# Kernel optimization log

Measured on AMD Instinct MI355X. Metric: run time of the kernel, lower is better.

Reference implementation:

```python
import jax, jax.numpy as jnp
import numpy as np

B, T, N, D, NH = 4, 256, 8, 128, 4
SCALES = (1, 2, 3, 5)
LAGS = (1, 2, 3)
MLP_H = 32
NL_SCALE = 0.1
CMIN, CMAX = -2.5, 2.0
L_ENC = 2  # num_attn_layers


def _ln(x, g, b, eps=1e-5):
    m = x.mean(-1, keepdims=True)
    v = ((x - m) ** 2).mean(-1, keepdims=True)
    return (x - m) * jax.lax.rsqrt(v + eps) * g + b


def _gelu(x):
    return jax.nn.gelu(x, approximate=False)


def _mha(q, k, v, Wq, bq, Wk, bk, Wv, bv, Wo, bo, nh):
    Bq, Lq, Dm = q.shape
    Lk = k.shape[1]
    hd = Dm // nh
    qh = (q @ Wq.T + bq).reshape(Bq, Lq, nh, hd).transpose(0, 2, 1, 3)
    kh = (k @ Wk.T + bk).reshape(Bq, Lk, nh, hd).transpose(0, 2, 1, 3)
    vh = (v @ Wv.T + bv).reshape(Bq, Lk, nh, hd).transpose(0, 2, 1, 3)
    s = jnp.einsum('bhqd,bhkd->bhqk', qh, kh) / jnp.sqrt(jnp.float32(hd))
    p = jax.nn.softmax(s, axis=-1)
    o = jnp.einsum('bhqk,bhkd->bhqd', p, vh).transpose(0, 2, 1, 3).reshape(Bq, Lq, Dm)
    return o @ Wo.T + bo


def setup_inputs() -> dict:
    key = jax.random.key(0)
    ks = jax.random.split(key, 24)
    def w(k, shape, s=0.02):
        return s * jax.random.normal(k, shape, jnp.float32)
    inp = {}
    inp['visible_states'] = jax.random.uniform(ks[0], (B, T, N), jnp.float32) + 0.05
    inp['state_emb'] = jax.random.normal(ks[1], (B, T, N, D), jnp.float32)
    # LearnedBaseline params
    inp['r5'] = 0.1 * jnp.ones((N,), jnp.float32)
    A = 0.02 * jax.random.normal(ks[2], (N, N), jnp.float32)
    inp['A55'] = A.at[jnp.arange(N), jnp.arange(N)].set(-0.2)
    inp['bl_bias'] = jnp.zeros((N,), jnp.float32)
    inp['nl_W1'] = w(ks[3], (MLP_H, N), 0.1); inp['nl_b1'] = jnp.zeros((MLP_H,), jnp.float32)
    inp['nl_W2'] = w(ks[4], (N, MLP_H), 0.1); inp['nl_b2'] = jnp.zeros((N,), jnp.float32)
    # ResidualEncoder input MLP
    IN_DIM = len(SCALES) * (1 + len(LAGS))  # 16
    inp['mlp_W1'] = w(ks[5], (D, IN_DIM), 0.1); inp['mlp_b1'] = jnp.zeros((D,), jnp.float32)
    inp['mlp_W2'] = w(ks[6], (D, D)); inp['mlp_b2'] = jnp.zeros((D,), jnp.float32)
    inp['mlp_ln_g'] = jnp.ones((D,), jnp.float32); inp['mlp_ln_b'] = jnp.zeros((D,), jnp.float32)
    # ResidualEncoder transformer layers (stacked over L_ENC layers)
    inp['enc_qkv_W'] = w(ks[7], (L_ENC, 3 * D, D)); inp['enc_qkv_b'] = jnp.zeros((L_ENC, 3 * D), jnp.float32)
    inp['enc_out_W'] = w(ks[8], (L_ENC, D, D)); inp['enc_out_b'] = jnp.zeros((L_ENC, D), jnp.float32)
    inp['enc_ln1_g'] = jnp.ones((L_ENC, D), jnp.float32); inp['enc_ln1_b'] = jnp.zeros((L_ENC, D), jnp.float32)
    inp['enc_ff_W1'] = w(ks[9], (L_ENC, 2 * D, D)); inp['enc_ff_b1'] = jnp.zeros((L_ENC, 2 * D), jnp.float32)
    inp['enc_ff_W2'] = w(ks[10], (L_ENC, D, 2 * D)); inp['enc_ff_b2'] = jnp.zeros((L_ENC, D), jnp.float32)
    inp['enc_ln2_g'] = jnp.ones((L_ENC, D), jnp.float32); inp['enc_ln2_b'] = jnp.zeros((L_ENC, D), jnp.float32)
    # CrossAttentionFusion
    inp['ca_Wq'] = w(ks[11], (D, D)); inp['ca_bq'] = jnp.zeros((D,), jnp.float32)
    inp['ca_Wk'] = w(ks[12], (D, D)); inp['ca_bk'] = jnp.zeros((D,), jnp.float32)
    inp['ca_Wv'] = w(ks[13], (D, D)); inp['ca_bv'] = jnp.zeros((D,), jnp.float32)
    inp['ca_Wo'] = w(ks[14], (D, D)); inp['ca_bo'] = jnp.zeros((D,), jnp.float32)
    inp['ca_ln1_g'] = jnp.ones((D,), jnp.float32); inp['ca_ln1_b'] = jnp.zeros((D,), jnp.float32)
    inp['ca_ff_W1'] = w(ks[15], (4 * D, 2 * D)); inp['ca_ff_b1'] = jnp.zeros((4 * D,), jnp.float32)
    inp['ca_ff_W2'] = w(ks[16], (D, 4 * D)); inp['ca_ff_b2'] = jnp.zeros((D,), jnp.float32)
    inp['ca_ln2_g'] = jnp.ones((D,), jnp.float32); inp['ca_ln2_b'] = jnp.zeros((D,), jnp.float32)
    return inp


def _forward(visible_states, state_emb, r5, A55, bl_bias, nl_W1, nl_b1, nl_W2, nl_b2,
             mlp_W1, mlp_b1, mlp_W2, mlp_b2, mlp_ln_g, mlp_ln_b,
             enc_qkv_W, enc_qkv_b, enc_out_W, enc_out_b, enc_ln1_g, enc_ln1_b,
             enc_ff_W1, enc_ff_b1, enc_ff_W2, enc_ff_b2, enc_ln2_g, enc_ln2_b,
             ca_Wq, ca_bq, ca_Wk, ca_bk, ca_Wv, ca_bv, ca_Wo, ca_bo,
             ca_ln1_g, ca_ln1_b, ca_ff_W1, ca_ff_b1, ca_ff_W2, ca_ff_b2,
             ca_ln2_g, ca_ln2_b):
    # ---- LearnedBaseline on x_t = visible_states[:, :-1] ----
    safe = jnp.clip(visible_states, 1e-6, None)
    logx = jnp.log(safe)
    x_t = visible_states[:, :-1]  # (B,T-1,N)
    lin = r5 + jnp.einsum('btn,mn->btm', x_t, A55)
    nl = _gelu(x_t @ nl_W1.T + nl_b1) @ nl_W2.T + nl_b2
    b1 = lin + NL_SCALE * nl + bl_bias  # (B,T-1,N)
    # ---- MultiScaleResidual ----
    res_list = []
    for k in SCALES:
        actual = jnp.clip(logx[:, k:] - logx[:, :-k], CMIN * k, CMAX * k)  # (B,T-k,N)
        bk = b1[:, 0:T - k]
        for i in range(1, k):
            bk = bk + b1[:, i:i + T - k]
        res = actual - bk
        res_list.append(jnp.pad(res, ((0, 0), (0, k), (0, 0))))
    residuals = jnp.stack(res_list, axis=-1)  # (B,T,N,S)
    # ---- ResidualEncoder: takens delays ----
    feats = [residuals] + [jnp.pad(residuals, ((0, 0), (lag, 0), (0, 0), (0, 0)))[:, :T]
                           for lag in LAGS]
    x = jnp.concatenate(feats, axis=-1)  # (B,T,N,16)
    x = _gelu(x @ mlp_W1.T + mlp_b1)
    x = _gelu(x @ mlp_W2.T + mlp_b2)
    x = _ln(x, mlp_ln_g, mlp_ln_b)
    # sinusoidal PE over time
    pos = jnp.arange(T, dtype=jnp.float32)[:, None]
    div = jnp.exp(jnp.arange(0, D, 2, dtype=jnp.float32) * (-jnp.log(10000.0) / D))
    pe = jnp.stack([jnp.sin(pos * div), jnp.cos(pos * div)], axis=-1).reshape(T, D)
    x = x + pe[None, :, None, :]
    # temporal self-attention over (B*N, T, D)
    xt = x.transpose(0, 2, 1, 3).reshape(B * N, T, D)
    for i in range(L_ENC):
        Wq, Wk, Wv = jnp.split(enc_qkv_W[i], 3, axis=0)
        bq, bk_, bv = jnp.split(enc_qkv_b[i], 3)
        a = _mha(xt, xt, xt, Wq, bq, Wk, bk_, Wv, bv, enc_out_W[i], enc_out_b[i], NH)
        xt = _ln(xt + a, enc_ln1_g[i], enc_ln1_b[i])
        ff = _gelu(xt @ enc_ff_W1[i].T + enc_ff_b1[i]) @ enc_ff_W2[i].T + enc_ff_b2[i]
        xt = _ln(xt + ff, enc_ln2_g[i], enc_ln2_b[i])
    residual_emb = xt.reshape(B, N, T, D).transpose(0, 2, 1, 3)  # (B,T,N,D)
    # ---- CrossAttentionFusion ----
    s = state_emb.reshape(B, T * N, D)
    r = residual_emb.reshape(B, T * N, D)
    a = _mha(s, r, r, ca_Wq, ca_bq, ca_Wk, ca_bk, ca_Wv, ca_bv, ca_Wo, ca_bo, NH)
    s = _ln(s + a, ca_ln1_g, ca_ln1_b)
    fused = _gelu(jnp.concatenate([s, r], axis=-1) @ ca_ff_W1.T + ca_ff_b1) @ ca_ff_W2.T + ca_ff_b2
    out = _ln(s + fused, ca_ln2_g, ca_ln2_b)
    return out.reshape(B, T, N, D)


def reference(visible_states, state_emb, r5, A55, bl_bias, nl_W1, nl_b1, nl_W2, nl_b2,
              mlp_W1, mlp_b1, mlp_W2, mlp_b2, mlp_ln_g, mlp_ln_b,
              enc_qkv_W, enc_qkv_b, enc_out_W, enc_out_b, enc_ln1_g, enc_ln1_b,
              enc_ff_W1, enc_ff_b1, enc_ff_W2, enc_ff_b2, enc_ln2_g, enc_ln2_b,
              ca_Wq, ca_bq, ca_Wk, ca_bk, ca_Wv, ca_bv, ca_Wo, ca_bo,
              ca_ln1_g, ca_ln1_b, ca_ff_W1, ca_ff_b1, ca_ff_W2, ca_ff_b2,
              ca_ln2_g, ca_ln2_b):
    return _forward(visible_states, state_emb, r5, A55, bl_bias, nl_W1, nl_b1, nl_W2, nl_b2,
                    mlp_W1, mlp_b1, mlp_W2, mlp_b2, mlp_ln_g, mlp_ln_b,
                    enc_qkv_W, enc_qkv_b, enc_out_W, enc_out_b, enc_ln1_g, enc_ln1_b,
                    enc_ff_W1, enc_ff_b1, enc_ff_W2, enc_ff_b2, enc_ln2_g, enc_ln2_b,
                    ca_Wq, ca_bq, ca_Wk, ca_bk, ca_Wv, ca_bv, ca_Wo, ca_bo,
                    ca_ln1_g, ca_ln1_b, ca_ff_W1, ca_ff_b1, ca_ff_W2, ca_ff_b2,
                    ca_ln2_g, ca_ln2_b)
```

## Files before the change

kernel.cpp:

```cpp
#include <hip/hip_runtime.h>
#include <math.h>

#define B_ 4
#define T_ 256
#define N_ 8
#define D_ 128
#define NH_ 4
#define HD_ 32
#define LENC_ 2
#define MLPH_ 32
#define NL_SCALE_ 0.1f

typedef __bf16 bf16;
typedef __attribute__((ext_vector_type(2))) __bf16 bf16x2;
typedef __attribute__((ext_vector_type(4))) __bf16 bf16x4;
typedef __attribute__((ext_vector_type(8))) __bf16 bf16x8;
typedef __attribute__((ext_vector_type(4))) float f32x4;

__device__ __forceinline__ f32x4 pv_mfma16(bf16x4 a, bf16x4 b, f32x4 c) {
#if __has_builtin(__builtin_amdgcn_mfma_f32_16x16x16_bf16)
    return __builtin_amdgcn_mfma_f32_16x16x16_bf16(a, b, c, 0, 0, 0);
#else
    typedef __attribute__((ext_vector_type(4))) short s4;
    union U { bf16x4 h; s4 s; };
    U ua, ub; ua.h = a; ub.h = b;
    return __builtin_amdgcn_mfma_f32_16x16x16bf16_1k(ua.s, ub.s, c, 0, 0, 0);
#endif
}

__device__ __forceinline__ float gelu_f(float x) {
    return 0.5f * x * (1.0f + erff(x * 0.7071067811865476f));
}

__global__ void k_prep_b1(const float* __restrict__ eqkvW, const float* __restrict__ eoutW,
                          const float* __restrict__ eff1, const float* __restrict__ eff2,
                          const float* __restrict__ wq, const float* __restrict__ wk,
                          const float* __restrict__ wv, const float* __restrict__ wo,
                          const float* __restrict__ cff1, const float* __restrict__ cff2,
                          const float* __restrict__ mlpW2, const float* __restrict__ semb,
                          const float* __restrict__ bk, const float* __restrict__ bv,
                          bf16* __restrict__ Wpk, bf16* __restrict__ sembh,
                          float* __restrict__ bpk,
                          const float* __restrict__ vs, const float* __restrict__ r5,
                          const float* __restrict__ A55, const float* __restrict__ bl_bias,
                          const float* __restrict__ nlW1, const float* __restrict__ nlb1,
                          const float* __restrict__ nlW2, const float* __restrict__ nlb2,
                          float* __restrict__ b1w) {
    if (blockIdx.x < 6209) {
        int i = blockIdx.x * 256 + threadIdx.x;
        if (i < 540672) {
            const float* src; int off;
            if      (i < 98304)  { src = eqkvW; off = 0; }
            else if (i < 131072) { src = eoutW; off = 98304; }
            else if (i < 196608) { src = eff1;  off = 131072; }
            else if (i < 262144) { src = eff2;  off = 196608; }
            else if (i < 278528) { src = wq;    off = 262144; }
            else if (i < 294912) { src = wk;    off = 278528; }
            else if (i < 311296) { src = wv;    off = 294912; }
            else if (i < 327680) { src = wo;    off = 311296; }
            else if (i < 458752) { src = cff1;  off = 327680; }
            else if (i < 524288) { src = cff2;  off = 458752; }
            else                 { src = mlpW2; off = 524288; }
            Wpk[i] = (bf16)src[i - off];
        } else if (i < 540672 + 1048576) {
            int j = i - 540672;
            sembh[j] = (bf16)semb[j];
        } else if (i < 540672 + 1048576 + 256) {
            int t = i - 540672 - 1048576;
            bpk[t] = (t < 128) ? bk[t] : bv[t - 128];
        }
        return;
    }
    int idx = (blockIdx.x - 6209) * 256 + threadIdx.x;
    if (idx >= B_ * (T_ - 1)) return;
    int b = idx / (T_ - 1), t = idx % (T_ - 1);
    float x[N_];
    for (int n = 0; n < N_; n++) x[n] = vs[(b * T_ + t) * N_ + n];
    float h[MLPH_];
    for (int j = 0; j < MLPH_; j++) {
        float a = nlb1[j];
        for (int n = 0; n < N_; n++) a += x[n] * nlW1[j * N_ + n];
        h[j] = gelu_f(a);
    }
    for (int m = 0; m < N_; m++) {
        float lin = r5[m];
        for (int n = 0; n < N_; n++) lin += x[n] * A55[m * N_ + n];
        float nl = nlb2[m];
        for (int j = 0; j < MLPH_; j++) nl += h[j] * nlW2[m * MLPH_ + j];
        b1w[idx * N_ + m] = lin + NL_SCALE_ * nl + bl_bias[m];
    }
}

__global__ __launch_bounds__(256) void k_mlp_ln(
    const float* __restrict__ vs, const float* __restrict__ b1w,
    const float* __restrict__ W1, const float* __restrict__ b1,
    const bf16* __restrict__ W2, const float* __restrict__ bias,
    const float* __restrict__ g, const float* __restrict__ be,
    float* __restrict__ outf, bf16* __restrict__ outh) {
    __shared__ float F[32][16];
    __shared__ bf16 H1[32][136];
    __shared__ float S[32][132];
    int tid = threadIdx.x;
    int blk = blockIdx.x;
#pragma unroll
    for (int e = tid; e < 512; e += 256) {
        int row = e >> 4, feat = e & 15;
        int grow = blk * 32 + row;
        int b = grow >> 11, t = (grow >> 3) & 255, n = grow & 7;
        const int SC[4] = {1, 2, 3, 5};
        int lag = feat >> 2, si = feat & 3, k = SC[si];
        int tp = t - lag;
        float r = 0.0f;
        if (tp >= 0 && tp < T_ - k) {
            float lx0 = logf(fmaxf(vs[(b * T_ + tp) * N_ + n], 1e-6f));
            float lx1 = logf(fmaxf(vs[(b * T_ + tp + k) * N_ + n], 1e-6f));
            float a = lx1 - lx0;
            a = fminf(fmaxf(a, -2.5f * (float)k), 2.0f * (float)k);
            float bk = 0.0f;
            for (int i = 0; i < k; i++) bk += b1w[(b * (T_ - 1) + tp + i) * N_ + n];
            r = a - bk;
        }
        F[row][feat] = r;
    }
    __syncthreads();
    {
        int row = tid >> 3, cg = tid & 7;
        float f[16];
#pragma unroll
        for (int c = 0; c < 16; c++) f[c] = F[row][c];
#pragma unroll
        for (int j = 0; j < 16; j++) {
            int d = cg * 16 + j;
            float a = b1[d];
            const float* w = W1 + d * 16;
#pragma unroll
            for (int c = 0; c < 16; c++) a += f[c] * w[c];
            H1[row][d] = (bf16)gelu_f(a);
        }
    }
    __syncthreads();
    int w = tid >> 6, lane = tid & 63;
    int c = lane & 15, gq = lane >> 4;
    int r0l = (w >> 1) * 16;
    int cb = (w & 1) * 64;
    const f32x4 zero = {0, 0, 0, 0};
    {
        const bf16x8* Wp0 = (const bf16x8*)(W2 + (size_t)(cb + c) * 128) + gq;
        const bf16x8* Wp1 = (const bf16x8*)(W2 + (size_t)(cb + 16 + c) * 128) + gq;
        const bf16x8* Wp2 = (const bf16x8*)(W2 + (size_t)(cb + 32 + c) * 128) + gq;
        const bf16x8* Wp3 = (const bf16x8*)(W2 + (size_t)(cb + 48 + c) * 128) + gq;
        f32x4 a0 = zero, a1 = zero, a2 = zero, a3 = zero;
#pragma unroll
        for (int k = 0; k < 4; k++) {
            bf16x8 av = *(const bf16x8*)&H1[r0l + c][k * 32 + gq * 8];
            a0 = __builtin_amdgcn_mfma_f32_16x16x32_bf16(av, Wp0[k * 4], a0, 0, 0, 0);
            a1 = __builtin_amdgcn_mfma_f32_16x16x32_bf16(av, Wp1[k * 4], a1, 0, 0, 0);
            a2 = __builtin_amdgcn_mfma_f32_16x16x32_bf16(av, Wp2[k * 4], a2, 0, 0, 0);
            a3 = __builtin_amdgcn_mfma_f32_16x16x32_bf16(av, Wp3[k * 4], a3, 0, 0, 0);
        }
        int lrow = r0l + gq * 4;
#pragma unroll
        for (int r = 0; r < 4; r++) {
            S[lrow + r][cb + c]      = gelu_f(a0[r] + bias[cb + c]);
            S[lrow + r][cb + 16 + c] = gelu_f(a1[r] + bias[cb + 16 + c]);
            S[lrow + r][cb + 32 + c] = gelu_f(a2[r] + bias[cb + 32 + c]);
            S[lrow + r][cb + 48 + c] = gelu_f(a3[r] + bias[cb + 48 + c]);
        }
    }
    __syncthreads();
    {
        int row = tid >> 3, cg = tid & 7;
        int grow = blk * 32 + row;
        int b = grow >> 11, t = (grow >> 3) & 255, n = grow & 7;
        int orow = (b * 8 + n) * 256 + t;
        float v[16];
#pragma unroll
        for (int j = 0; j < 16; j++) v[j] = S[row][cg * 16 + j];
        float s = 0.0f;
#pragma unroll
        for (int j = 0; j < 16; j++) s += v[j];
        s += __shfl_xor(s, 1); s += __shfl_xor(s, 2); s += __shfl_xor(s, 4);
        float mean = s * (1.0f / 128.0f);
        float vs2 = 0.0f;
#pragma unroll
        for (int j = 0; j < 16; j++) { float d = v[j] - mean; vs2 += d * d; }
        vs2 += __shfl_xor(vs2, 1); vs2 += __shfl_xor(vs2, 2); vs2 += __shfl_xor(vs2, 4);
        float rstd = rsqrtf(vs2 * (1.0f / 128.0f) + 1e-5f);
        float y[16];
#pragma unroll
        for (int j = 0; j < 16; j++) {
            int col = cg * 16 + j;
            y[j] = (v[j] - mean) * rstd * g[col] + be[col];
        }
#pragma unroll
        for (int jj = 0; jj < 8; jj++) {
            int j2 = cg * 8 + jj;
            float freq = expf((float)(2 * j2) * (-9.210340371976184f / 128.0f));
            float ang = (float)t * freq;
            y[2 * jj] += sinf(ang);
            y[2 * jj + 1] += cosf(ang);
        }
        float4* of = (float4*)(outf + (size_t)orow * 128 + cg * 16);
        bf16x8* oh = (bf16x8*)(outh + (size_t)orow * 128 + cg * 16);
#pragma unroll
        for (int j4 = 0; j4 < 4; j4++) {
            float4 o; o.x = y[4 * j4]; o.y = y[4 * j4 + 1];
            o.z = y[4 * j4 + 2]; o.w = y[4 * j4 + 3];
            of[j4] = o;
        }
#pragma unroll
        for (int j8 = 0; j8 < 2; j8++) {
            bf16x8 o;
#pragma unroll
            for (int e = 0; e < 8; e++) o[e] = (bf16)y[8 * j8 + e];
            oh[j8] = o;
        }
    }
}

__global__ __launch_bounds__(256) void k_enc_attn(
    const bf16* __restrict__ X0h, const bf16* __restrict__ Wqkv,
    const float* __restrict__ bqkv, bf16* __restrict__ ATTh) {
    int sh = blockIdx.x;
    int s = sh >> 2, h = sh & 3;
    __shared__ bf16 Ql[256][40];
    __shared__ bf16 Kl[256][40];
    __shared__ bf16 Vt[32][264];
    int tid = threadIdx.x;
    int wv = tid >> 6, lane = tid & 63;
    int c = lane & 15, g = lane >> 4;
    const f32x4 zero = {0, 0, 0, 0};

    {
        const bf16* Wq0 = Wqkv + (size_t)(h * 32 + c) * 128;
        const bf16* Wq1 = Wqkv + (size_t)(h * 32 + 16 + c) * 128;
        const bf16* Wk0 = Wqkv + (size_t)(128 + h * 32 + c) * 128;
        const bf16* Wk1 = Wqkv + (size_t)(128 + h * 32 + 16 + c) * 128;
        const bf16* Wv0 = Wqkv + (size_t)(256 + h * 32 + c) * 128;
        const bf16* Wv1 = Wqkv + (size_t)(256 + h * 32 + 16 + c) * 128;
        float bq0 = bqkv[h * 32 + c], bq1 = bqkv[h * 32 + 16 + c];
        float bk0 = bqkv[128 + h * 32 + c], bk1 = bqkv[128 + h * 32 + 16 + c];
        float bv0 = bqkv[256 + h * 32 + c], bv1 = bqkv[256 + h * 32 + 16 + c];
#pragma unroll
        for (int rb = 0; rb < 4; rb++) {
            int row0 = wv * 64 + rb * 16;
            const bf16x8* Ap = (const bf16x8*)(X0h + (size_t)(s * 256 + row0 + c) * 128) + g;
            f32x4 aq0 = zero, aq1 = zero, ak0 = zero, ak1 = zero, av0 = zero, av1 = zero;
#pragma unroll
            for (int k = 0; k < 4; k++) {
                bf16x8 av = Ap[k * 4];
                aq0 = __builtin_amdgcn_mfma_f32_16x16x32_bf16(av, *((const bf16x8*)Wq0 + k * 4 + g), aq0, 0, 0, 0);
                aq1 = __builtin_amdgcn_mfma_f32_16x16x32_bf16(av, *((const bf16x8*)Wq1 + k * 4 + g), aq1, 0, 0, 0);
                ak0 = __builtin_amdgcn_mfma_f32_16x16x32_bf16(av, *((const bf16x8*)Wk0 + k * 4 + g), ak0, 0, 0, 0);
                ak1 = __builtin_amdgcn_mfma_f32_16x16x32_bf16(av, *((const bf16x8*)Wk1 + k * 4 + g), ak1, 0, 0, 0);
                av0 = __builtin_amdgcn_mfma_f32_16x16x32_bf16(av, *((const bf16x8*)Wv0 + k * 4 + g), av0, 0, 0, 0);
                av1 = __builtin_amdgcn_mfma_f32_16x16x32_bf16(av, *((const bf16x8*)Wv1 + k * 4 + g), av1, 0, 0, 0);
            }
            int lr = row0 + g * 4;
#pragma unroll
            for (int i = 0; i < 4; i++) {
                Ql[lr + i][c] = (bf16)(aq0[i] + bq0);
                Ql[lr + i][16 + c] = (bf16)(aq1[i] + bq1);
                Kl[lr + i][c] = (bf16)(ak0[i] + bk0);
                Kl[lr + i][16 + c] = (bf16)(ak1[i] + bk1);
                Vt[c][lr + i] = (bf16)(av0[i] + bv0);
                Vt[16 + c][lr + i] = (bf16)(av1[i] + bv1);
            }
        }
    }
    __syncthreads();

    const float scale = 0.17677669529663687f;
    int q0 = wv * 64;
    bf16x8 bq[4];
#pragma unroll
    for (int qt = 0; qt < 4; qt++)
        bq[qt] = *(const bf16x8*)&Ql[q0 + qt * 16 + c][g * 8];
    f32x4 oT[4][2];
#pragma unroll
    for (int qt = 0; qt < 4; qt++) { oT[qt][0] = zero; oT[qt][1] = zero; }
    float lsum[4] = {0, 0, 0, 0};
#pragma unroll
    for (int t = 0; t < 8; t++) {
        int k0 = t * 32;
        bf16x8 ka = *(const bf16x8*)&Kl[k0 + c][g * 8];
        bf16x8 kb = *(const bf16x8*)&Kl[k0 + 16 + c][g * 8];
        bf16x4 va0 = *(const bf16x4*)&Vt[c][k0 + g * 4];
        bf16x4 va1 = *(const bf16x4*)&Vt[c][k0 + 16 + g * 4];
        bf16x4 vb0 = *(const bf16x4*)&Vt[16 + c][k0 + g * 4];
        bf16x4 vb1 = *(const bf16x4*)&Vt[16 + c][k0 + 16 + g * 4];
#pragma unroll
        for (int qt = 0; qt < 4; qt++) {
            f32x4 s0 = __builtin_amdgcn_mfma_f32_16x16x32_bf16(ka, bq[qt], zero, 0, 0, 0);
            f32x4 s1 = __builtin_amdgcn_mfma_f32_16x16x32_bf16(kb, bq[qt], zero, 0, 0, 0);
            bf16x4 p0, p1;
#pragma unroll
            for (int r = 0; r < 4; r++) {
                float e0 = __expf(s0[r] * scale);
                float e1 = __expf(s1[r] * scale);
                lsum[qt] += e0 + e1;
                p0[r] = (bf16)e0;
                p1[r] = (bf16)e1;
            }
            oT[qt][0] = pv_mfma16(va0, p0, oT[qt][0]);
            oT[qt][0] = pv_mfma16(va1, p1, oT[qt][0]);
            oT[qt][1] = pv_mfma16(vb0, p0, oT[qt][1]);
            oT[qt][1] = pv_mfma16(vb1, p1, oT[qt][1]);
        }
    }
#pragma unroll
    for (int qt = 0; qt < 4; qt++) {
        float sm = lsum[qt];
        sm += __shfl_xor(sm, 16);
        sm += __shfl_xor(sm, 32);
        float inv = 1.0f / sm;
        size_t rbase = ((size_t)s * 256 + q0 + qt * 16 + c) * 128 + h * 32;
#pragma unroll
        for (int r = 0; r < 4; r++) {
            ATTh[rbase + g * 4 + r] = (bf16)(oT[qt][0][r] * inv);
            ATTh[rbase + 16 + g * 4 + r] = (bf16)(oT[qt][1][r] * inv);
        }
    }
}

__device__ __forceinline__ void gemm4_body(
    int bid, const bf16* __restrict__ A, const bf16* __restrict__ W,
    const float* __restrict__ bias, bf16* __restrict__ dq,
    bf16* __restrict__ dk, bf16* __restrict__ dvv, int N, int K, int mode) {
    int lane = threadIdx.x & 63;
    int wv = threadIdx.x >> 6;
    int c = lane & 15, g = lane >> 4;
    int nN = N >> 6;
    int tn = bid % nN, tm = bid / nN;
    int row0 = tm * 64 + wv * 16;
    int cb = tn * 64;

    const bf16x8* Ap  = (const bf16x8*)(A + (size_t)(row0 + c) * K) + g;
    const bf16x8* Wp0 = (const bf16x8*)(W + (size_t)(cb + c) * K) + g;
    const bf16x8* Wp1 = (const bf16x8*)(W + (size_t)(cb + 16 + c) * K) + g;
    const bf16x8* Wp2 = (const bf16x8*)(W + (size_t)(cb + 32 + c) * K) + g;
    const bf16x8* Wp3 = (const bf16x8*)(W + (size_t)(cb + 48 + c) * K) + g;
    f32x4 a0 = {0, 0, 0, 0}, a1 = {0, 0, 0, 0};
    f32x4 a2 = {0, 0, 0, 0}, a3 = {0, 0, 0, 0};
    int nk = K >> 5;
    for (int k = 0; k < nk; k++) {
        bf16x8 av = Ap[k * 4];
        a0 = __builtin_amdgcn_mfma_f32_16x16x32_bf16(av, Wp0[k * 4], a0, 0, 0, 0);
        a1 = __builtin_amdgcn_mfma_f32_16x16x32_bf16(av, Wp1[k * 4], a1, 0, 0, 0);
        a2 = __builtin_amdgcn_mfma_f32_16x16x32_bf16(av, Wp2[k * 4], a2, 0, 0, 0);
        a3 = __builtin_amdgcn_mfma_f32_16x16x32_bf16(av, Wp3[k * 4], a3, 0, 0, 0);
    }
    int rowb = row0 + g * 4;
#pragma unroll
    for (int ct = 0; ct < 4; ct++) {
        f32x4 acc = (ct == 0) ? a0 : (ct == 1) ? a1 : (ct == 2) ? a2 : a3;
        int col = cb + ct * 16 + c;
        float bvv = bias[col];
#pragma unroll
        for (int i = 0; i < 4; i++) {
            float v = acc[i] + bvv;
            int row = rowb + i;
            if (mode == 2) {
                int b = row >> 11, ll = row & 2047;
                int hh = col >> 5, d = col & 31;
                dq[((size_t)(b * 4 + hh) * 2048 + ll) * 32 + d] = (bf16)v;
            } else {
                int b = row >> 11, n = (row >> 8) & 7, t = row & 255;
                int ll = t * 8 + n;
                int hh = (col >> 5) & 3, d = col & 31;
                if (col < 128) dk[((size_t)(b * 4 + hh) * 2048 + ll) * 32 + d] = (bf16)v;
                else           dvv[((size_t)(b * 4 + hh) * 32 + d) * 2048 + ll] = (bf16)v;
            }
        }
    }
}

__global__ __launch_bounds__(256) void k_qkvc(
    const bf16* __restrict__ sembh, const bf16* __restrict__ Wq,
    const float* __restrict__ bq, const bf16* __restrict__ X0h,
    const bf16* __restrict__ Wkv, const float* __restrict__ bkv,
    bf16* __restrict__ Qh, bf16* __restrict__ Kh, bf16* __restrict__ Vth) {
    if (blockIdx.x < 256)
        gemm4_body(blockIdx.x, sembh, Wq, bq, Qh, nullptr, nullptr, 128, 128, 2);
    else
        gemm4_body(blockIdx.x - 256, X0h, Wkv, bkv, nullptr, Kh, Vth, 256, 128, 3);
}

__global__ __launch_bounds__(256) void k_enc_tail(
    const bf16* __restrict__ ATTh, const bf16* __restrict__ Wo,
    const float* __restrict__ bo, const float* __restrict__ X0res,
    const float* __restrict__ g1, const float* __restrict__ be1,
    const bf16* __restrict__ W1, const float* __restrict__ bf1,
    const bf16* __restrict__ W2, const float* __restrict__ bf2,
    const float* __restrict__ g2, const float* __restrict__ be2,
    float* __restrict__ X0out, bf16* __restrict__ X0hout) {
    __shared__ float S[32][132];
    __shared__ float X1f[32][132];
    __shared__ bf16 X1h[32][136];
    __shared__ bf16 H[32][264];
    int tid = threadIdx.x;
    int w = tid >> 6, lane = tid & 63;
    int c = lane & 15, gq = lane >> 4;
    int r0l = (w >> 1) * 16;
    int cb = (w & 1) * 64;
    int blk = blockIdx.x;
    const f32x4 zero = {0, 0, 0, 0};

    {
        const bf16x8* Ap  = (const bf16x8*)(ATTh + (size_t)(blk * 32 + r0l + c) * 128) + gq;
        const bf16x8* Wp0 = (const bf16x8*)(Wo + (size_t)(cb + c) * 128) + gq;
        const bf16x8* Wp1 = (const bf16x8*)(Wo + (size_t)(cb + 16 + c) * 128) + gq;
        const bf16x8* Wp2 = (const bf16x8*)(Wo + (size_t)(cb + 32 + c) * 128) + gq;
        const bf16x8* Wp3 = (const bf16x8*)(Wo + (size_t)(cb + 48 + c) * 128) + gq;
        f32x4 a0 = zero, a1 = zero, a2 = zero, a3 = zero;
#pragma unroll
        for (int k = 0; k < 4; k++) {
            bf16x8 av = Ap[k * 4];
            a0 = __builtin_amdgcn_mfma_f32_16x16x32_bf16(av, Wp0[k * 4], a0, 0, 0, 0);
            a1 = __builtin_amdgcn_mfma_f32_16x16x32_bf16(av, Wp1[k * 4], a1, 0, 0, 0);
            a2 = __builtin_amdgcn_mfma_f32_16x16x32_bf16(av, Wp2[k * 4], a2, 0, 0, 0);
            a3 = __builtin_amdgcn_mfma_f32_16x16x32_bf16(av, Wp3[k * 4], a3, 0, 0, 0);
        }
        int lrow = r0l + gq * 4;
        float b0 = bo[cb + c], b1v = bo[cb + 16 + c];
        float b2v = bo[cb + 32 + c], b3v = bo[cb + 48 + c];
#pragma unroll
        for (int r = 0; r < 4; r++) {
            S[lrow + r][cb + c] = a0[r] + b0;
            S[lrow + r][cb + 16 + c] = a1[r] + b1v;
            S[lrow + r][cb + 32 + c] = a2[r] + b2v;
            S[lrow + r][cb + 48 + c] = a3[r] + b3v;
        }
    }
    __syncthreads();
    {
        int row = tid >> 3, cg = tid & 7;
        float v[16];
        const float4* rp = (const float4*)(X0res + (size_t)(blk * 32 + row) * 128 + cg * 16);
#pragma unroll
        for (int j4 = 0; j4 < 4; j4++) {
            float4 rv = rp[j4];
            v[4 * j4 + 0] = S[row][cg * 16 + 4 * j4 + 0] + rv.x;
            v[4 * j4 + 1] = S[row][cg * 16 + 4 * j4 + 1] + rv.y;
            v[4 * j4 + 2] = S[row][cg * 16 + 4 * j4 + 2] + rv.z;
            v[4 * j4 + 3] = S[row][cg * 16 + 4 * j4 + 3] + rv.w;
        }
        float s = 0.0f;
#pragma unroll
        for (int j = 0; j < 16; j++) s += v[j];
        s += __shfl_xor(s, 1); s += __shfl_xor(s, 2); s += __shfl_xor(s, 4);
        float mean = s * (1.0f / 128.0f);
        float vs = 0.0f;
#pragma unroll
        for (int j = 0; j < 16; j++) { float d = v[j] - mean; vs += d * d; }
        vs += __shfl_xor(vs, 1); vs += __shfl_xor(vs, 2); vs += __shfl_xor(vs, 4);
        float rstd = rsqrtf(vs * (1.0f / 128.0f) + 1e-5f);
#pragma unroll
        for (int j = 0; j < 16; j++) {
            int col = cg * 16 + j;
            float y = (v[j] - mean) * rstd * g1[col] + be1[col];
            X1f[row][col] = y;
            X1h[row][col] = (bf16)y;
        }
    }
    __syncthreads();
    {
        bf16x8 af[4];
#pragma unroll
        for (int k = 0; k < 4; k++)
            af[k] = *(const bf16x8*)&X1h[r0l + c][k * 32 + gq * 8];
#pragma unroll
        for (int ci = 0; ci < 2; ci++) {
            int cb2 = cb + ci * 128;
            const bf16x8* Wp0 = (const bf16x8*)(W1 + (size_t)(cb2 + c) * 128) + gq;
            const bf16x8* Wp1 = (const bf16x8*)(W1 + (size_t)(cb2 + 16 + c) * 128) + gq;
            const bf16x8* Wp2 = (const bf16x8*)(W1 + (size_t)(cb2 + 32 + c) * 128) + gq;
            const bf16x8* Wp3 = (const bf16x8*)(W1 + (size_t)(cb2 + 48 + c) * 128) + gq;
            f32x4 a0 = zero, a1 = zero, a2 = zero, a3 = zero;
#pragma unroll
            for (int k = 0; k < 4; k++) {
                a0 = __builtin_amdgcn_mfma_f32_16x16x32_bf16(af[k], Wp0[k * 4], a0, 0, 0, 0);
                a1 = __builtin_amdgcn_mfma_f32_16x16x32_bf16(af[k], Wp1[k * 4], a1, 0, 0, 0);
                a2 = __builtin_amdgcn_mfma_f32_16x16x32_bf16(af[k], Wp2[k * 4], a2, 0, 0, 0);
                a3 = __builtin_amdgcn_mfma_f32_16x16x32_bf16(af[k], Wp3[k * 4], a3, 0, 0, 0);
            }
            int lrow = r0l + gq * 4;
#pragma unroll
            for (int r = 0; r < 4; r++) {
                H[lrow + r][cb2 + c]      = (bf16)gelu_f(a0[r] + bf1[cb2 + c]);
                H[lrow + r][cb2 + 16 + c] = (bf16)gelu_f(a1[r] + bf1[cb2 + 16 + c]);
                H[lrow + r][cb2 + 32 + c] = (bf16)gelu_f(a2[r] + bf1[cb2 + 32 + c]);
                H[lrow + r][cb2 + 48 + c] = (bf16)gelu_f(a3[r] + bf1[cb2 + 48 + c]);
            }
        }
    }
    __syncthreads();
    {
        bf16x8 af[8];
#pragma unroll
        for (int k = 0; k < 8; k++)
            af[k] = *(const bf16x8*)&H[r0l + c][k * 32 + gq * 8];
        const bf16x8* Wp0 = (const bf16x8*)(W2 + (size_t)(cb + c) * 256) + gq;
        const bf16x8* Wp1 = (const bf16x8*)(W2 + (size_t)(cb + 16 + c) * 256) + gq;
        const bf16x8* Wp2 = (const bf16x8*)(W2 + (size_t)(cb + 32 + c) * 256) + gq;
        const bf16x8* Wp3 = (const bf16x8*)(W2 + (size_t)(cb + 48 + c) * 256) + gq;
        f32x4 a0 = zero, a1 = zero, a2 = zero, a3 = zero;
#pragma unroll
        for (int k = 0; k < 8; k++) {
            a0 = __builtin_amdgcn_mfma_f32_16x16x32_bf16(af[k], Wp0[k * 4], a0, 0, 0, 0);
            a1 = __builtin_amdgcn_mfma_f32_16x16x32_bf16(af[k], Wp1[k * 4], a1, 0, 0, 0);
            a2 = __builtin_amdgcn_mfma_f32_16x16x32_bf16(af[k], Wp2[k * 4], a2, 0, 0, 0);
            a3 = __builtin_amdgcn_mfma_f32_16x16x32_bf16(af[k], Wp3[k * 4], a3, 0, 0, 0);
        }
        int lrow = r0l + gq * 4;
        float b0 = bf2[cb + c], b1v = bf2[cb + 16 + c];
        float b2v = bf2[cb + 32 + c], b3v = bf2[cb + 48 + c];
#pragma unroll
        for (int r = 0; r < 4; r++) {
            S[lrow + r][cb + c] = a0[r] + b0;
            S[lrow + r][cb + 16 + c] = a1[r] + b1v;
            S[lrow + r][cb + 32 + c] = a2[r] + b2v;
            S[lrow + r][cb + 48 + c] = a3[r] + b3v;
        }
    }
    __syncthreads();
    {
        int row = tid >> 3, cg = tid & 7;
        float v[16];
#pragma unroll
        for (int j = 0; j < 16; j++)
            v[j] = S[row][cg * 16 + j] + X1f[row][cg * 16 + j];
        float s = 0.0f;
#pragma unroll
        for (int j = 0; j < 16; j++) s += v[j];
        s += __shfl_xor(s, 1); s += __shfl_xor(s, 2); s += __shfl_xor(s, 4);
        float mean = s * (1.0f / 128.0f);
        float vs = 0.0f;
#pragma unroll
        for (int j = 0; j < 16; j++) { float d = v[j] - mean; vs += d * d; }
        vs += __shfl_xor(vs, 1); vs += __shfl_xor(vs, 2); vs += __shfl_xor(vs, 4);
        float rstd = rsqrtf(vs * (1.0f / 128.0f) + 1e-5f);
        size_t grow = (size_t)(blk * 32 + row);
        float4* of = (float4*)(X0out + grow * 128 + cg * 16);
        bf16x8* oh = (bf16x8*)(X0hout + grow * 128 + cg * 16);
        float y[16];
#pragma unroll
        for (int j = 0; j < 16; j++) {
            int col = cg * 16 + j;
            y[j] = (v[j] - mean) * rstd * g2[col] + be2[col];
        }
#pragma unroll
        for (int j4 = 0; j4 < 4; j4++) {
            float4 o; o.x = y[4 * j4]; o.y = y[4 * j4 + 1];
            o.z = y[4 * j4 + 2]; o.w = y[4 * j4 + 3];
            of[j4] = o;
        }
#pragma unroll
        for (int j8 = 0; j8 < 2; j8++) {
            bf16x8 o;
#pragma unroll
            for (int e = 0; e < 8; e++) o[e] = (bf16)y[8 * j8 + e];
            oh[j8] = o;
        }
    }
}

__global__ __launch_bounds__(256) void k_cross_tail(
    const bf16* __restrict__ ATTh, const bf16* __restrict__ Wo,
    const float* __restrict__ bo, const float* __restrict__ semb,
    const float* __restrict__ g1, const float* __restrict__ be1,
    const bf16* __restrict__ X0h, const bf16* __restrict__ W1,
    const float* __restrict__ bf1, const bf16* __restrict__ W2,
    const float* __restrict__ bf2, const float* __restrict__ g2,
    const float* __restrict__ be2, float* __restrict__ outp) {
    __shared__ float S[32][132];
    __shared__ bf16 s1h[32][136];
    __shared__ bf16 H[32][520];
    int tid = threadIdx.x;
    int w = tid >> 6, lane = tid & 63;
    int c = lane & 15, gq = lane >> 4;
    int r0l = (w >> 1) * 16;
    int cb = (w & 1) * 64;
    int blk = blockIdx.x;
    const f32x4 zero = {0, 0, 0, 0};

    bf16x8 agl[4];
    {
        int tr = blk * 32 + r0l + c;
        int b = tr >> 11, t = (tr >> 3) & 255, n = tr & 7;
        const bf16* xrow = X0h + ((size_t)((b * 8 + n) * 256 + t)) * 128;
#pragma unroll
        for (int k = 0; k < 4; k++)
            agl[k] = *(const bf16x8*)(xrow + k * 32 + gq * 8);
    }

    {
        const bf16x8* Ap  = (const bf16x8*)(ATTh + (size_t)(blk * 32 + r0l + c) * 128) + gq;
        const bf16x8* Wp0 = (const bf16x8*)(Wo + (size_t)(cb + c) * 128) + gq;
        const bf16x8* Wp1 = (const bf16x8*)(Wo + (size_t)(cb + 16 + c) * 128) + gq;
        const bf16x8* Wp2 = (const bf16x8*)(Wo + (size_t)(cb + 32 + c) * 128) + gq;
        const bf16x8* Wp3 = (const bf16x8*)(Wo + (size_t)(cb + 48 + c) * 128) + gq;
        f32x4 a0 = zero, a1 = zero, a2 = zero, a3 = zero;
#pragma unroll
        for (int k = 0; k < 4; k++) {
            bf16x8 av = Ap[k * 4];
            a0 = __builtin_amdgcn_mfma_f32_16x16x32_bf16(av, Wp0[k * 4], a0, 0, 0, 0);
            a1 = __builtin_amdgcn_mfma_f32_16x16x32_bf16(av, Wp1[k * 4], a1, 0, 0, 0);
            a2 = __builtin_amdgcn_mfma_f32_16x16x32_bf16(av, Wp2[k * 4], a2, 0, 0, 0);
            a3 = __builtin_amdgcn_mfma_f32_16x16x32_bf16(av, Wp3[k * 4], a3, 0, 0, 0);
        }
        int lrow = r0l + gq * 4;
        float b0 = bo[cb + c], b1v = bo[cb + 16 + c];
        float b2v = bo[cb + 32 + c], b3v = bo[cb + 48 + c];
#pragma unroll
        for (int r = 0; r < 4; r++) {
            S[lrow + r][cb + c] = a0[r] + b0;
            S[lrow + r][cb + 16 + c] = a1[r] + b1v;
            S[lrow + r][cb + 32 + c] = a2[r] + b2v;
            S[lrow + r][cb + 48 + c] = a3[r] + b3v;
        }
    }
    __syncthreads();
    {
        int row = tid >> 3, cg = tid & 7;
        float v[16];
        const float4* rp = (const float4*)(semb + (size_t)(blk * 32 + row) * 128 + cg * 16);
#pragma unroll
        for (int j4 = 0; j4 < 4; j4++) {
            float4 rv = rp[j4];
            v[4 * j4 + 0] = S[row][cg * 16 + 4 * j4 + 0] + rv.x;
            v[4 * j4 + 1] = S[row][cg * 16 + 4 * j4 + 1] + rv.y;
            v[4 * j4 + 2] = S[row][cg * 16 + 4 * j4 + 2] + rv.z;
            v[4 * j4 + 3] = S[row][cg * 16 + 4 * j4 + 3] + rv.w;
        }
        float s = 0.0f;
#pragma unroll
        for (int j = 0; j < 16; j++) s += v[j];
        s += __shfl_xor(s, 1); s += __shfl_xor(s, 2); s += __shfl_xor(s, 4);
        float mean = s * (1.0f / 128.0f);
        float vs = 0.0f;
#pragma unroll
        for (int j = 0; j < 16; j++) { float d = v[j] - mean; vs += d * d; }
        vs += __shfl_xor(vs, 1); vs += __shfl_xor(vs, 2); vs += __shfl_xor(vs, 4);
        float rstd = rsqrtf(vs * (1.0f / 128.0f) + 1e-5f);
#pragma unroll
        for (int j = 0; j < 16; j++) {
            int col = cg * 16 + j;
            s1h[row][col] = (bf16)((v[j] - mean) * rstd * g1[col] + be1[col]);
        }
    }
    __syncthreads();
    {
        bf16x8 afl[4];
#pragma unroll
        for (int k = 0; k < 4; k++)
            afl[k] = *(const bf16x8*)&s1h[r0l + c][k * 32 + gq * 8];
#pragma unroll
        for (int ci = 0; ci < 4; ci++) {
            int cb2 = cb + ci * 128;
            const bf16x8* Wp0 = (const bf16x8*)(W1 + (size_t)(cb2 + c) * 256) + gq;
            const bf16x8* Wp1 = (const bf16x8*)(W1 + (size_t)(cb2 + 16 + c) * 256) + gq;
            const bf16x8* Wp2 = (const bf16x8*)(W1 + (size_t)(cb2 + 32 + c) * 256) + gq;
            const bf16x8* Wp3 = (const bf16x8*)(W1 + (size_t)(cb2 + 48 + c) * 256) + gq;
            f32x4 a0 = zero, a1 = zero, a2 = zero, a3 = zero;
#pragma unroll
            for (int k = 0; k < 8; k++) {
                bf16x8 av = (k < 4) ? afl[k] : agl[k - 4];
                a0 = __builtin_amdgcn_mfma_f32_16x16x32_bf16(av, Wp0[k * 4], a0, 0, 0, 0);
                a1 = __builtin_amdgcn_mfma_f32_16x16x32_bf16(av, Wp1[k * 4], a1, 0, 0, 0);
                a2 = __builtin_amdgcn_mfma_f32_16x16x32_bf16(av, Wp2[k * 4], a2, 0, 0, 0);
                a3 = __builtin_amdgcn_mfma_f32_16x16x32_bf16(av, Wp3[k * 4], a3, 0, 0, 0);
            }
            int lrow = r0l + gq * 4;
#pragma unroll
            for (int r = 0; r < 4; r++) {
                H[lrow + r][cb2 + c]      = (bf16)gelu_f(a0[r] + bf1[cb2 + c]);
                H[lrow + r][cb2 + 16 + c] = (bf16)gelu_f(a1[r] + bf1[cb2 + 16 + c]);
                H[lrow + r][cb2 + 32 + c] = (bf16)gelu_f(a2[r] + bf1[cb2 + 32 + c]);
                H[lrow + r][cb2 + 48 + c] = (bf16)gelu_f(a3[r] + bf1[cb2 + 48 + c]);
            }
        }
    }
    __syncthreads();
    {
        const bf16x8* Wp0 = (const bf16x8*)(W2 + (size_t)(cb + c) * 512) + gq;
        const bf16x8* Wp1 = (const bf16x8*)(W2 + (size_t)(cb + 16 + c) * 512) + gq;
        const bf16x8* Wp2 = (const bf16x8*)(W2 + (size_t)(cb + 32 + c) * 512) + gq;
        const bf16x8* Wp3 = (const bf16x8*)(W2 + (size_t)(cb + 48 + c) * 512) + gq;
        f32x4 a0 = zero, a1 = zero, a2 = zero, a3 = zero;
#pragma unroll
        for (int k = 0; k < 16; k++) {
            bf16x8 av = *(const bf16x8*)&H[r0l + c][k * 32 + gq * 8];
            a0 = __builtin_amdgcn_mfma_f32_16x16x32_bf16(av, Wp0[k * 4], a0, 0, 0, 0);
            a1 = __builtin_amdgcn_mfma_f32_16x16x32_bf16(av, Wp1[k * 4], a1, 0, 0, 0);
            a2 = __builtin_amdgcn_mfma_f32_16x16x32_bf16(av, Wp2[k * 4], a2, 0, 0, 0);
            a3 = __builtin_amdgcn_mfma_f32_16x16x32_bf16(av, Wp3[k * 4], a3, 0, 0, 0);
        }
        int lrow = r0l + gq * 4;
        float b0 = bf2[cb + c], b1v = bf2[cb + 16 + c];
        float b2v = bf2[cb + 32 + c], b3v = bf2[cb + 48 + c];
#pragma unroll
        for (int r = 0; r < 4; r++) {
            S[lrow + r][cb + c] = a0[r] + b0;
            S[lrow + r][cb + 16 + c] = a1[r] + b1v;
            S[lrow + r][cb + 32 + c] = a2[r] + b2v;
            S[lrow + r][cb + 48 + c] = a3[r] + b3v;
        }
    }
    __syncthreads();
    {
        int row = tid >> 3, cg = tid & 7;
        float v[16];
#pragma unroll
        for (int j = 0; j < 16; j++)
            v[j] = S[row][cg * 16 + j] + (float)s1h[row][cg * 16 + j];
        float s = 0.0f;
#pragma unroll
        for (int j = 0; j < 16; j++) s += v[j];
        s += __shfl_xor(s, 1); s += __shfl_xor(s, 2); s += __shfl_xor(s, 4);
        float mean = s * (1.0f / 128.0f);
        float vs = 0.0f;
#pragma unroll
        for (int j = 0; j < 16; j++) { float d = v[j] - mean; vs += d * d; }
        vs += __shfl_xor(vs, 1); vs += __shfl_xor(vs, 2); vs += __shfl_xor(vs, 4);
        float rstd = rsqrtf(vs * (1.0f / 128.0f) + 1e-5f);
        float4* of = (float4*)(outp + (size_t)(blk * 32 + row) * 128 + cg * 16);
#pragma unroll
        for (int j4 = 0; j4 < 4; j4++) {
            float4 o;
#pragma unroll
            for (int e = 0; e < 4; e++) {
                int col = cg * 16 + 4 * j4 + e;
                ((float*)&o)[e] = (v[4 * j4 + e] - mean) * rstd * g2[col] + be2[col];
            }
            of[j4] = o;
        }
    }
}

__global__ __launch_bounds__(256) void k_mattn(
    const bf16* __restrict__ Qh, const bf16* __restrict__ Kh,
    const bf16* __restrict__ Vth, bf16* __restrict__ ATTh,
    int Lq, int Lk, int NSH) {
    int sh = blockIdx.x % NSH;
    int qblk = blockIdx.x / NSH;
    int wv = threadIdx.x >> 6;
    int lane = threadIdx.x & 63;
    int c = lane & 15, g = lane >> 4;
    int q0 = qblk * 64;

    __shared__ float O_lds[4][64][36];
    __shared__ float L_lds[4][64];

    const float scale = 0.17677669529663687f;
    const f32x4 zero = {0, 0, 0, 0};

    bf16x8 bq[4];
#pragma unroll
    for (int qt = 0; qt < 4; qt++)
        bq[qt] = *(const bf16x8*)(
            Qh + ((size_t)sh * Lq + q0 + qt * 16 + c) * 32 + g * 8);

    int klen = Lk >> 2;
    int kbeg = wv * klen;
    const bf16* Kbase = Kh + (size_t)sh * Lk * 32 + (size_t)kbeg * 32;
    const bf16* Vbase = Vth + (size_t)sh * 32 * Lk + kbeg;

    f32x4 oT[4][2];
#pragma unroll
    for (int qt = 0; qt < 4; qt++) { oT[qt][0] = zero; oT[qt][1] = zero; }
    float lsum[4] = {0, 0, 0, 0};

    int ntiles = klen >> 5;
    bf16x8 ka = *(const bf16x8*)(Kbase + (size_t)c * 32 + g * 8);
    bf16x8 kb = *(const bf16x8*)(Kbase + (size_t)(16 + c) * 32 + g * 8);
    bf16x4 va0 = *(const bf16x4*)(Vbase + (size_t)c * Lk + g * 4);
    bf16x4 va1 = *(const bf16x4*)(Vbase + (size_t)c * Lk + 16 + g * 4);
    bf16x4 vb0 = *(const bf16x4*)(Vbase + (size_t)(16 + c) * Lk + g * 4);
    bf16x4 vb1 = *(const bf16x4*)(Vbase + (size_t)(16 + c) * Lk + 16 + g * 4);

    for (int t = 0; t < ntiles; t++) {
        bf16x8 cka = ka, ckb = kb;
        bf16x4 cva0 = va0, cva1 = va1, cvb0 = vb0, cvb1 = vb1;
        int nk0 = ((t + 1 < ntiles) ? (t + 1) : t) << 5;
        ka = *(const bf16x8*)(Kbase + (size_t)(nk0 + c) * 32 + g * 8);
        kb = *(const bf16x8*)(Kbase + (size_t)(nk0 + 16 + c) * 32 + g * 8);
        va0 = *(const bf16x4*)(Vbase + (size_t)c * Lk + nk0 + g * 4);
        va1 = *(const bf16x4*)(Vbase + (size_t)c * Lk + nk0 + 16 + g * 4);
        vb0 = *(const bf16x4*)(Vbase + (size_t)(16 + c) * Lk + nk0 + g * 4);
        vb1 = *(const bf16x4*)(Vbase + (size_t)(16 + c) * Lk + nk0 + 16 + g * 4);

#pragma unroll
        for (int qt = 0; qt < 4; qt++) {
            f32x4 s0 = __builtin_amdgcn_mfma_f32_16x16x32_bf16(cka, bq[qt], zero, 0, 0, 0);
            f32x4 s1 = __builtin_amdgcn_mfma_f32_16x16x32_bf16(ckb, bq[qt], zero, 0, 0, 0);
            bf16x4 p0, p1;
#pragma unroll
            for (int r = 0; r < 4; r++) {
                float e0 = __expf(s0[r] * scale);
                float e1 = __expf(s1[r] * scale);
                lsum[qt] += e0 + e1;
                p0[r] = (bf16)e0;
                p1[r] = (bf16)e1;
            }
            oT[qt][0] = pv_mfma16(cva0, p0, oT[qt][0]);
            oT[qt][0] = pv_mfma16(cva1, p1, oT[qt][0]);
            oT[qt][1] = pv_mfma16(cvb0, p0, oT[qt][1]);
            oT[qt][1] = pv_mfma16(cvb1, p1, oT[qt][1]);
        }
    }

#pragma unroll
    for (int qt = 0; qt < 4; qt++) {
        float s = lsum[qt];
        s += __shfl_xor(s, 16);
        s += __shfl_xor(s, 32);
        if (g == 0) L_lds[wv][qt * 16 + c] = s;
        *(f32x4*)&O_lds[wv][qt * 16 + c][g * 4] = oT[qt][0];
        *(f32x4*)&O_lds[wv][qt * 16 + c][16 + g * 4] = oT[qt][1];
    }
    __syncthreads();

    int tid = threadIdx.x;
    int ql = tid >> 2, dq = (tid & 3) * 8;
    float ltot = L_lds[0][ql] + L_lds[1][ql] + L_lds[2][ql] + L_lds[3][ql];
    float inv = 1.0f / ltot;
    float acc[8];
#pragma unroll
    for (int j = 0; j < 8; j++) acc[j] = 0.0f;
#pragma unroll
    for (int w = 0; w < 4; w++) {
        const float* p = &O_lds[w][ql][dq];
#pragma unroll
        for (int j = 0; j < 8; j++) acc[j] += p[j];
    }
    int h = sh & 3, sb = sh >> 2;
    bf16x8 o;
#pragma unroll
    for (int j = 0; j < 8; j++) o[j] = (bf16)(acc[j] * inv);
    *(bf16x8*)(ATTh + ((size_t)sb * Lq + q0 + ql) * 128 + h * 32 + dq) = o;
}

extern "C" void kernel_launch(void* const* d_in, const int* in_sizes, int n_in,
                              void* d_out, int out_size, void* d_ws, size_t ws_size,
                              hipStream_t stream) {
    const float* vs       = (const float*)d_in[0];
    const float* semb     = (const float*)d_in[1];
    const float* r5       = (const float*)d_in[2];
    const float* A55      = (const float*)d_in[3];
    const float* bl_bias  = (const float*)d_in[4];
    const float* nl_W1    = (const float*)d_in[5];
    const float* nl_b1    = (const float*)d_in[6];
    const float* nl_W2    = (const float*)d_in[7];
    const float* nl_b2    = (const float*)d_in[8];
    const float* mlp_W1   = (const float*)d_in[9];
    const float* mlp_b1   = (const float*)d_in[10];
    const float* mlp_W2   = (const float*)d_in[11];
    const float* mlp_b2   = (const float*)d_in[12];
    const float* mlp_ln_g = (const float*)d_in[13];
    const float* mlp_ln_b = (const float*)d_in[14];
    const float* enc_qkv_W = (const float*)d_in[15];
    const float* enc_qkv_b = (const float*)d_in[16];
    const float* enc_out_W = (const float*)d_in[17];
    const float* enc_out_b = (const float*)d_in[18];
    const float* enc_ln1_g = (const float*)d_in[19];
    const float* enc_ln1_b = (const float*)d_in[20];
    const float* enc_ff_W1 = (const float*)d_in[21];
    const float* enc_ff_b1 = (const float*)d_in[22];
    const float* enc_ff_W2 = (const float*)d_in[23];
    const float* enc_ff_b2 = (const float*)d_in[24];
    const float* enc_ln2_g = (const float*)d_in[25];
    const float* enc_ln2_b = (const float*)d_in[26];
    const float* ca_Wq = (const float*)d_in[27];
    const float* ca_bq = (const float*)d_in[28];
    const float* ca_Wk = (const float*)d_in[29];
    const float* ca_bk = (const float*)d_in[30];
    const float* ca_Wv = (const float*)d_in[31];
    const float* ca_bv = (const float*)d_in[32];
    const float* ca_Wo = (const float*)d_in[33];
    const float* ca_bo = (const float*)d_in[34];
    const float* ca_ln1_g = (const float*)d_in[35];
    const float* ca_ln1_b = (const float*)d_in[36];
    const float* ca_ff_W1 = (const float*)d_in[37];
    const float* ca_ff_b1 = (const float*)d_in[38];
    const float* ca_ff_W2 = (const float*)d_in[39];
    const float* ca_ff_b2 = (const float*)d_in[40];
    const float* ca_ln2_g = (const float*)d_in[41];
    const float* ca_ln2_b = (const float*)d_in[42];
    float* out = (float*)d_out;

    char* base = (char*)d_ws;
    float* b1w   = (float*)(base + 0);
    float* X0    = (float*)(base + 163840);
    char*  QKVr  = base + 8552448;
    bf16*  Wpk   = (bf16*) (base + 25329664);
    float* bpk   = (float*)(base + 26411008);
    bf16*  X0h   = (bf16*) (base + 26412032);
    bf16*  sembh = (bf16*) (base + 30606336);
    bf16*  ATTh  = (bf16*) (base + 32703488);
    bf16*  Qh    = (bf16*)QKVr;
    bf16*  Kh    = (bf16*)(QKVr + 2097152);
    bf16*  Vth   = (bf16*)(QKVr + 4194304);

    k_prep_b1<<<dim3(6213), dim3(256), 0, stream>>>(
        enc_qkv_W, enc_out_W, enc_ff_W1, enc_ff_W2, ca_Wq, ca_Wk, ca_Wv, ca_Wo,
        ca_ff_W1, ca_ff_W2, mlp_W2, semb, ca_bk, ca_bv, Wpk, sembh, bpk,
        vs, r5, A55, bl_bias, nl_W1, nl_b1, nl_W2, nl_b2, b1w);

    k_mlp_ln<<<dim3(256), dim3(256), 0, stream>>>(
        vs, b1w, mlp_W1, mlp_b1, Wpk + 524288, mlp_b2, mlp_ln_g, mlp_ln_b,
        X0, X0h);

    for (int i = 0; i < LENC_; i++) {
        k_enc_attn<<<dim3(128), dim3(256), 0, stream>>>(
            X0h, Wpk + i * 49152, enc_qkv_b + i * 384, ATTh);
        k_enc_tail<<<dim3(256), dim3(256), 0, stream>>>(
            ATTh, Wpk + 98304 + i * 16384, enc_out_b + i * 128, X0,
            enc_ln1_g + i * 128, enc_ln1_b + i * 128,
            Wpk + 131072 + i * 32768, enc_ff_b1 + i * 256,
            Wpk + 196608 + i * 32768, enc_ff_b2 + i * 128,
            enc_ln2_g + i * 128, enc_ln2_b + i * 128, X0, X0h);
    }

    k_qkvc<<<dim3(768), dim3(256), 0, stream>>>(
        sembh, Wpk + 262144, ca_bq, X0h, Wpk + 278528, bpk, Qh, Kh, Vth);
    k_mattn<<<dim3(512), dim3(256), 0, stream>>>(
        Qh, Kh, Vth, ATTh, 2048, 2048, 16);
    k_cross_tail<<<dim3(256), dim3(256), 0, stream>>>(
        ATTh, Wpk + 311296, ca_bo, semb, ca_ln1_g, ca_ln1_b, X0h,
        Wpk + 327680, ca_ff_b1, Wpk + 458752, ca_ff_b2,
        ca_ln2_g, ca_ln2_b, out);
}
```

Before: 337.1 us.

## Halve rows per block in MLP/tail kernels and split encoder attention queries

The row-wise kernels (input MLP+LN, encoder tail, cross tail) now handle 16 rows per block instead of 32, so twice as many blocks are launched and each wave owns a 32-column slice. Encoder attention is split into two query halves per (sequence, head), doubling its grid. The aim is to fill more of the GPU's compute units, since 128–256 blocks underuse the device. In exchange, every block reloads the same weights, and each attention block recomputes the full K/V projection, which doubles that work.

```diff
diff --git a/kernel.cpp b/kernel.cpp
--- a/kernel.cpp
+++ b/kernel.cpp
@@ -97,15 +97,14 @@
     const bf16* __restrict__ W2, const float* __restrict__ bias,
     const float* __restrict__ g, const float* __restrict__ be,
     float* __restrict__ outf, bf16* __restrict__ outh) {
-    __shared__ float F[32][16];
-    __shared__ bf16 H1[32][136];
-    __shared__ float S[32][132];
+    __shared__ float F[16][16];
+    __shared__ bf16 H1[16][136];
+    __shared__ float S[16][132];
     int tid = threadIdx.x;
     int blk = blockIdx.x;
-#pragma unroll
-    for (int e = tid; e < 512; e += 256) {
-        int row = e >> 4, feat = e & 15;
-        int grow = blk * 32 + row;
+    {
+        int row = tid >> 4, feat = tid & 15;
+        int grow = blk * 16 + row;
         int b = grow >> 11, t = (grow >> 3) & 255, n = grow & 7;
         const int SC[4] = {1, 2, 3, 5};
         int lag = feat >> 2, si = feat & 3, k = SC[si];
@@ -124,13 +123,13 @@
     }
     __syncthreads();
     {
-        int row = tid >> 3, cg = tid & 7;
+        int row = tid >> 4, cg = tid & 15;
         float f[16];
 #pragma unroll
         for (int c = 0; c < 16; c++) f[c] = F[row][c];
 #pragma unroll
-        for (int j = 0; j < 16; j++) {
-            int d = cg * 16 + j;
+        for (int j = 0; j < 8; j++) {
+            int d = cg * 8 + j;
             float a = b1[d];
             const float* w = W1 + d * 16;
 #pragma unroll
@@ -141,89 +140,76 @@
     __syncthreads();
     int w = tid >> 6, lane = tid & 63;
     int c = lane & 15, gq = lane >> 4;
-    int r0l = (w >> 1) * 16;
-    int cb = (w & 1) * 64;
+    int cb = w * 32;
     const f32x4 zero = {0, 0, 0, 0};
     {
         const bf16x8* Wp0 = (const bf16x8*)(W2 + (size_t)(cb + c) * 128) + gq;
         const bf16x8* Wp1 = (const bf16x8*)(W2 + (size_t)(cb + 16 + c) * 128) + gq;
-        const bf16x8* Wp2 = (const bf16x8*)(W2 + (size_t)(cb + 32 + c) * 128) + gq;
-        const bf16x8* Wp3 = (const bf16x8*)(W2 + (size_t)(cb + 48 + c) * 128) + gq;
-        f32x4 a0 = zero, a1 = zero, a2 = zero, a3 = zero;
+        f32x4 a0 = zero, a1 = zero;
 #pragma unroll
         for (int k = 0; k < 4; k++) {
-            bf16x8 av = *(const bf16x8*)&H1[r0l + c][k * 32 + gq * 8];
+            bf16x8 av = *(const bf16x8*)&H1[c][k * 32 + gq * 8];
             a0 = __builtin_amdgcn_mfma_f32_16x16x32_bf16(av, Wp0[k * 4], a0, 0, 0, 0);
             a1 = __builtin_amdgcn_mfma_f32_16x16x32_bf16(av, Wp1[k * 4], a1, 0, 0, 0);
-            a2 = __builtin_amdgcn_mfma_f32_16x16x32_bf16(av, Wp2[k * 4], a2, 0, 0, 0);
-            a3 = __builtin_amdgcn_mfma_f32_16x16x32_bf16(av, Wp3[k * 4], a3, 0, 0, 0);
-        }
-        int lrow = r0l + gq * 4;
+        }
 #pragma unroll
         for (int r = 0; r < 4; r++) {
-            S[lrow + r][cb + c]      = gelu_f(a0[r] + bias[cb + c]);
-            S[lrow + r][cb + 16 + c] = gelu_f(a1[r] + bias[cb + 16 + c]);
-            S[lrow + r][cb + 32 + c] = gelu_f(a2[r] + bias[cb + 32 + c]);
-            S[lrow + r][cb + 48 + c] = gelu_f(a3[r] + bias[cb + 48 + c]);
-        }
-    }
-    __syncthreads();
-    {
-        int row = tid >> 3, cg = tid & 7;
-        int grow = blk * 32 + row;
+            S[gq * 4 + r][cb + c]      = gelu_f(a0[r] + bias[cb + c]);
+            S[gq * 4 + r][cb + 16 + c] = gelu_f(a1[r] + bias[cb + 16 + c]);
+        }
+    }
+    __syncthreads();
+    {
+        int row = tid >> 4, cg = tid & 15;
+        int grow = blk * 16 + row;
         int b = grow >> 11, t = (grow >> 3) & 255, n = grow & 7;
         int orow = (b * 8 + n) * 256 + t;
-        float v[16];
-#pragma unroll
-        for (int j = 0; j < 16; j++) v[j] = S[row][cg * 16 + j];
+        float v[8];
+#pragma unroll
+        for (int j = 0; j < 8; j++) v[j] = S[row][cg * 8 + j];
         float s = 0.0f;
 #pragma unroll
-        for (int j = 0; j < 16; j++) s += v[j];
-        s += __shfl_xor(s, 1); s += __shfl_xor(s, 2); s += __shfl_xor(s, 4);
+        for (int j = 0; j < 8; j++) s += v[j];
+        s += __shfl_xor(s, 1); s += __shfl_xor(s, 2);
+        s += __shfl_xor(s, 4); s += __shfl_xor(s, 8);
         float mean = s * (1.0f / 128.0f);
         float vs2 = 0.0f;
 #pragma unroll
-        for (int j = 0; j < 16; j++) { float d = v[j] - mean; vs2 += d * d; }
-        vs2 += __shfl_xor(vs2, 1); vs2 += __shfl_xor(vs2, 2); vs2 += __shfl_xor(vs2, 4);
+        for (int j = 0; j < 8; j++) { float d = v[j] - mean; vs2 += d * d; }
+        vs2 += __shfl_xor(vs2, 1); vs2 += __shfl_xor(vs2, 2);
+        vs2 += __shfl_xor(vs2, 4); vs2 += __shfl_xor(vs2, 8);
         float rstd = rsqrtf(vs2 * (1.0f / 128.0f) + 1e-5f);
-        float y[16];
-#pragma unroll
-        for (int j = 0; j < 16; j++) {
-            int col = cg * 16 + j;
+        float y[8];
+#pragma unroll
+        for (int j = 0; j < 8; j++) {
+            int col = cg * 8 + j;
             y[j] = (v[j] - mean) * rstd * g[col] + be[col];
         }
 #pragma unroll
-        for (int jj = 0; jj < 8; jj++) {
-            int j2 = cg * 8 + jj;
+        for (int jj = 0; jj < 4; jj++) {
+            int j2 = cg * 4 + jj;
             float freq = expf((float)(2 * j2) * (-9.210340371976184f / 128.0f));
             float ang = (float)t * freq;
             y[2 * jj] += sinf(ang);
             y[2 * jj + 1] += cosf(ang);
         }
-        float4* of = (float4*)(outf + (size_t)orow * 128 + cg * 16);
-        bf16x8* oh = (bf16x8*)(outh + (size_t)orow * 128 + cg * 16);
-#pragma unroll
-        for (int j4 = 0; j4 < 4; j4++) {
-            float4 o; o.x = y[4 * j4]; o.y = y[4 * j4 + 1];
-            o.z = y[4 * j4 + 2]; o.w = y[4 * j4 + 3];
-            of[j4] = o;
-        }
-#pragma unroll
-        for (int j8 = 0; j8 < 2; j8++) {
-            bf16x8 o;
-#pragma unroll
-            for (int e = 0; e < 8; e++) o[e] = (bf16)y[8 * j8 + e];
-            oh[j8] = o;
-        }
+        float4* of = (float4*)(outf + (size_t)orow * 128 + cg * 8);
+        of[0] = (float4){y[0], y[1], y[2], y[3]};
+        of[1] = (float4){y[4], y[5], y[6], y[7]};
+        bf16x8 o;
+#pragma unroll
+        for (int e = 0; e < 8; e++) o[e] = (bf16)y[e];
+        *(bf16x8*)(outh + (size_t)orow * 128 + cg * 8) = o;
     }
 }
 
 __global__ __launch_bounds__(256) void k_enc_attn(
     const bf16* __restrict__ X0h, const bf16* __restrict__ Wqkv,
     const float* __restrict__ bqkv, bf16* __restrict__ ATTh) {
-    int sh = blockIdx.x;
+    int sh = blockIdx.x & 127;
+    int qh = blockIdx.x >> 7;
     int s = sh >> 2, h = sh & 3;
-    __shared__ bf16 Ql[256][40];
+    __shared__ bf16 Ql[128][40];
     __shared__ bf16 Kl[256][40];
     __shared__ bf16 Vt[32][264];
     int tid = threadIdx.x;
@@ -231,55 +217,69 @@
     int c = lane & 15, g = lane >> 4;
     const f32x4 zero = {0, 0, 0, 0};
 
-    {
-        const bf16* Wq0 = Wqkv + (size_t)(h * 32 + c) * 128;
-        const bf16* Wq1 = Wqkv + (size_t)(h * 32 + 16 + c) * 128;
-        const bf16* Wk0 = Wqkv + (size_t)(128 + h * 32 + c) * 128;
-        const bf16* Wk1 = Wqkv + (size_t)(128 + h * 32 + 16 + c) * 128;
-        const bf16* Wv0 = Wqkv + (size_t)(256 + h * 32 + c) * 128;
-        const bf16* Wv1 = Wqkv + (size_t)(256 + h * 32 + 16 + c) * 128;
-        float bq0 = bqkv[h * 32 + c], bq1 = bqkv[h * 32 + 16 + c];
-        float bk0 = bqkv[128 + h * 32 + c], bk1 = bqkv[128 + h * 32 + 16 + c];
-        float bv0 = bqkv[256 + h * 32 + c], bv1 = bqkv[256 + h * 32 + 16 + c];
-#pragma unroll
-        for (int rb = 0; rb < 4; rb++) {
-            int row0 = wv * 64 + rb * 16;
-            const bf16x8* Ap = (const bf16x8*)(X0h + (size_t)(s * 256 + row0 + c) * 128) + g;
-            f32x4 aq0 = zero, aq1 = zero, ak0 = zero, ak1 = zero, av0 = zero, av1 = zero;
-#pragma unroll
-            for (int k = 0; k < 4; k++) {
-                bf16x8 av = Ap[k * 4];
-                aq0 = __builtin_amdgcn_mfma_f32_16x16x32_bf16(av, *((const bf16x8*)Wq0 + k * 4 + g), aq0, 0, 0, 0);
-                aq1 = __builtin_amdgcn_mfma_f32_16x16x32_bf16(av, *((const bf16x8*)Wq1 + k * 4 + g), aq1, 0, 0, 0);
-                ak0 = __builtin_amdgcn_mfma_f32_16x16x32_bf16(av, *((const bf16x8*)Wk0 + k * 4 + g), ak0, 0, 0, 0);
-                ak1 = __builtin_amdgcn_mfma_f32_16x16x32_bf16(av, *((const bf16x8*)Wk1 + k * 4 + g), ak1, 0, 0, 0);
-                av0 = __builtin_amdgcn_mfma_f32_16x16x32_bf16(av, *((const bf16x8*)Wv0 + k * 4 + g), av0, 0, 0, 0);
-                av1 = __builtin_amdgcn_mfma_f32_16x16x32_bf16(av, *((const bf16x8*)Wv1 + k * 4 + g), av1, 0, 0, 0);
-            }
-            int lr = row0 + g * 4;
-#pragma unroll
-            for (int i = 0; i < 4; i++) {
-                Ql[lr + i][c] = (bf16)(aq0[i] + bq0);
-                Ql[lr + i][16 + c] = (bf16)(aq1[i] + bq1);
-                Kl[lr + i][c] = (bf16)(ak0[i] + bk0);
-                Kl[lr + i][16 + c] = (bf16)(ak1[i] + bk1);
-                Vt[c][lr + i] = (bf16)(av0[i] + bv0);
-                Vt[16 + c][lr + i] = (bf16)(av1[i] + bv1);
-            }
+    const bf16* Wq0 = Wqkv + (size_t)(h * 32 + c) * 128;
+    const bf16* Wq1 = Wqkv + (size_t)(h * 32 + 16 + c) * 128;
+    const bf16* Wk0 = Wqkv + (size_t)(128 + h * 32 + c) * 128;
+    const bf16* Wk1 = Wqkv + (size_t)(128 + h * 32 + 16 + c) * 128;
+    const bf16* Wv0 = Wqkv + (size_t)(256 + h * 32 + c) * 128;
+    const bf16* Wv1 = Wqkv + (size_t)(256 + h * 32 + 16 + c) * 128;
+    float bq0 = bqkv[h * 32 + c], bq1 = bqkv[h * 32 + 16 + c];
+    float bk0 = bqkv[128 + h * 32 + c], bk1 = bqkv[128 + h * 32 + 16 + c];
+    float bv0 = bqkv[256 + h * 32 + c], bv1 = bqkv[256 + h * 32 + 16 + c];
+
+#pragma unroll
+    for (int rb = 0; rb < 4; rb++) {
+        int row0 = wv * 64 + rb * 16;
+        const bf16x8* Ap = (const bf16x8*)(X0h + (size_t)(s * 256 + row0 + c) * 128) + g;
+        f32x4 ak0 = zero, ak1 = zero, av0 = zero, av1 = zero;
+#pragma unroll
+        for (int k = 0; k < 4; k++) {
+            bf16x8 av = Ap[k * 4];
+            ak0 = __builtin_amdgcn_mfma_f32_16x16x32_bf16(av, *((const bf16x8*)Wk0 + k * 4 + g), ak0, 0, 0, 0);
+            ak1 = __builtin_amdgcn_mfma_f32_16x16x32_bf16(av, *((const bf16x8*)Wk1 + k * 4 + g), ak1, 0, 0, 0);
+            av0 = __builtin_amdgcn_mfma_f32_16x16x32_bf16(av, *((const bf16x8*)Wv0 + k * 4 + g), av0, 0, 0, 0);
+            av1 = __builtin_amdgcn_mfma_f32_16x16x32_bf16(av, *((const bf16x8*)Wv1 + k * 4 + g), av1, 0, 0, 0);
+        }
+        int lr = row0 + g * 4;
+#pragma unroll
+        for (int i = 0; i < 4; i++) {
+            Kl[lr + i][c] = (bf16)(ak0[i] + bk0);
+            Kl[lr + i][16 + c] = (bf16)(ak1[i] + bk1);
+            Vt[c][lr + i] = (bf16)(av0[i] + bv0);
+            Vt[16 + c][lr + i] = (bf16)(av1[i] + bv1);
+        }
+    }
+#pragma unroll
+    for (int qb = 0; qb < 2; qb++) {
+        int row0q = wv * 32 + qb * 16;
+        const bf16x8* Ap = (const bf16x8*)(
+            X0h + (size_t)(s * 256 + qh * 128 + row0q + c) * 128) + g;
+        f32x4 aq0 = zero, aq1 = zero;
+#pragma unroll
+        for (int k = 0; k < 4; k++) {
+            bf16x8 av = Ap[k * 4];
+            aq0 = __builtin_amdgcn_mfma_f32_16x16x32_bf16(av, *((const bf16x8*)Wq0 + k * 4 + g), aq0, 0, 0, 0);
+            aq1 = __builtin_amdgcn_mfma_f32_16x16x32_bf16(av, *((const bf16x8*)Wq1 + k * 4 + g), aq1, 0, 0, 0);
+        }
+        int lr = row0q + g * 4;
+#pragma unroll
+        for (int i = 0; i < 4; i++) {
+            Ql[lr + i][c] = (bf16)(aq0[i] + bq0);
+            Ql[lr + i][16 + c] = (bf16)(aq1[i] + bq1);
         }
     }
     __syncthreads();
 
     const float scale = 0.17677669529663687f;
-    int q0 = wv * 64;
-    bf16x8 bq[4];
-#pragma unroll
-    for (int qt = 0; qt < 4; qt++)
-        bq[qt] = *(const bf16x8*)&Ql[q0 + qt * 16 + c][g * 8];
-    f32x4 oT[4][2];
-#pragma unroll
-    for (int qt = 0; qt < 4; qt++) { oT[qt][0] = zero; oT[qt][1] = zero; }
-    float lsum[4] = {0, 0, 0, 0};
+    int q0l = wv * 32;
+    bf16x8 bq[2];
+#pragma unroll
+    for (int qt = 0; qt < 2; qt++)
+        bq[qt] = *(const bf16x8*)&Ql[q0l + qt * 16 + c][g * 8];
+    f32x4 oT[2][2];
+#pragma unroll
+    for (int qt = 0; qt < 2; qt++) { oT[qt][0] = zero; oT[qt][1] = zero; }
+    float lsum[2] = {0, 0};
 #pragma unroll
     for (int t = 0; t < 8; t++) {
         int k0 = t * 32;
@@ -290,7 +290,7 @@
         bf16x4 vb0 = *(const bf16x4*)&Vt[16 + c][k0 + g * 4];
         bf16x4 vb1 = *(const bf16x4*)&Vt[16 + c][k0 + 16 + g * 4];
 #pragma unroll
-        for (int qt = 0; qt < 4; qt++) {
+        for (int qt = 0; qt < 2; qt++) {
             f32x4 s0 = __builtin_amdgcn_mfma_f32_16x16x32_bf16(ka, bq[qt], zero, 0, 0, 0);
             f32x4 s1 = __builtin_amdgcn_mfma_f32_16x16x32_bf16(kb, bq[qt], zero, 0, 0, 0);
             bf16x4 p0, p1;
@@ -309,12 +309,12 @@
         }
     }
 #pragma unroll
-    for (int qt = 0; qt < 4; qt++) {
+    for (int qt = 0; qt < 2; qt++) {
         float sm = lsum[qt];
         sm += __shfl_xor(sm, 16);
         sm += __shfl_xor(sm, 32);
         float inv = 1.0f / sm;
-        size_t rbase = ((size_t)s * 256 + q0 + qt * 16 + c) * 128 + h * 32;
+        size_t rbase = ((size_t)s * 256 + qh * 128 + q0l + qt * 16 + c) * 128 + h * 32;
 #pragma unroll
         for (int r = 0; r < 4; r++) {
             ATTh[rbase + g * 4 + r] = (bf16)(oT[qt][0][r] * inv);
@@ -394,70 +394,59 @@
     const bf16* __restrict__ W2, const float* __restrict__ bf2,
     const float* __restrict__ g2, const float* __restrict__ be2,
     float* __restrict__ X0out, bf16* __restrict__ X0hout) {
-    __shared__ float S[32][132];
-    __shared__ float X1f[32][132];
-    __shared__ bf16 X1h[32][136];
-    __shared__ bf16 H[32][264];
+    __shared__ float S[16][132];
+    __shared__ float X1f[16][132];
+    __shared__ bf16 X1h[16][136];
+    __shared__ bf16 H[16][264];
     int tid = threadIdx.x;
     int w = tid >> 6, lane = tid & 63;
     int c = lane & 15, gq = lane >> 4;
-    int r0l = (w >> 1) * 16;
-    int cb = (w & 1) * 64;
     int blk = blockIdx.x;
     const f32x4 zero = {0, 0, 0, 0};
 
     {
-        const bf16x8* Ap  = (const bf16x8*)(ATTh + (size_t)(blk * 32 + r0l + c) * 128) + gq;
+        int cb = w * 32;
+        const bf16x8* Ap  = (const bf16x8*)(ATTh + (size_t)(blk * 16 + c) * 128) + gq;
         const bf16x8* Wp0 = (const bf16x8*)(Wo + (size_t)(cb + c) * 128) + gq;
         const bf16x8* Wp1 = (const bf16x8*)(Wo + (size_t)(cb + 16 + c) * 128) + gq;
-        const bf16x8* Wp2 = (const bf16x8*)(Wo + (size_t)(cb + 32 + c) * 128) + gq;
-        const bf16x8* Wp3 = (const bf16x8*)(Wo + (size_t)(cb + 48 + c) * 128) + gq;
-        f32x4 a0 = zero, a1 = zero, a2 = zero, a3 = zero;
+        f32x4 a0 = zero, a1 = zero;
 #pragma unroll
         for (int k = 0; k < 4; k++) {
             bf16x8 av = Ap[k * 4];
             a0 = __builtin_amdgcn_mfma_f32_16x16x32_bf16(av, Wp0[k * 4], a0, 0, 0, 0);
             a1 = __builtin_amdgcn_mfma_f32_16x16x32_bf16(av, Wp1[k * 4], a1, 0, 0, 0);
-            a2 = __builtin_amdgcn_mfma_f32_16x16x32_bf16(av, Wp2[k * 4], a2, 0, 0, 0);
-            a3 = __builtin_amdgcn_mfma_f32_16x16x32_bf16(av, Wp3[k * 4], a3, 0, 0, 0);
-        }
-        int lrow = r0l + gq * 4;
-        float b0 = bo[cb + c], b1v = bo[cb + 16 + c];
-        float b2v = bo[cb + 32 + c], b3v = bo[cb + 48 + c];
+        }
 #pragma unroll
         for (int r = 0; r < 4; r++) {
-            S[lrow + r][cb + c] = a0[r] + b0;
-            S[lrow + r][cb + 16 + c] = a1[r] + b1v;
-            S[lrow + r][cb + 32 + c] = a2[r] + b2v;
-            S[lrow + r][cb + 48 + c] = a3[r] + b3v;
-        }
-    }
-    __syncthreads();
-    {
-        int row = tid >> 3, cg = tid & 7;
-        float v[16];
-        const float4* rp = (const float4*)(X0res + (size_t)(blk * 32 + row) * 128 + cg * 16);
-#pragma unroll
-        for (int j4 = 0; j4 < 4; j4++) {
-            float4 rv = rp[j4];
-            v[4 * j4 + 0] = S[row][cg * 16 + 4 * j4 + 0] + rv.x;
-            v[4 * j4 + 1] = S[row][cg * 16 + 4 * j4 + 1] + rv.y;
-            v[4 * j4 + 2] = S[row][cg * 16 + 4 * j4 + 2] + rv.z;
-            v[4 * j4 + 3] = S[row][cg * 16 + 4 * j4 + 3] + rv.w;
-        }
+            S[gq * 4 + r][cb + c] = a0[r] + bo[cb + c];
+            S[gq * 4 + r][cb + 16 + c] = a1[r] + bo[cb + 16 + c];
+        }
+    }
+    __syncthreads();
+    {
+        int row = tid >> 4, cg = tid & 15;
+        float v[8];
+        const float4* rp = (const float4*)(X0res + (size_t)(blk * 16 + row) * 128 + cg * 8);
+        float4 r0 = rp[0], r1 = rp[1];
+        v[0] = S[row][cg * 8 + 0] + r0.x; v[1] = S[row][cg * 8 + 1] + r0.y;
+        v[2] = S[row][cg * 8 + 2] + r0.z; v[3] = S[row][cg * 8 + 3] + r0.w;
+        v[4] = S[row][cg * 8 + 4] + r1.x; v[5] = S[row][cg * 8 + 5] + r1.y;
+        v[6] = S[row][cg * 8 + 6] + r1.z; v[7] = S[row][cg * 8 + 7] + r1.w;
         float s = 0.0f;
 #pragma unroll
-        for (int j = 0; j < 16; j++) s += v[j];
-        s += __shfl_xor(s, 1); s += __shfl_xor(s, 2); s += __shfl_xor(s, 4);
+        for (int j = 0; j < 8; j++) s += v[j];
+        s += __shfl_xor(s, 1); s += __shfl_xor(s, 2);
+        s += __shfl_xor(s, 4); s += __shfl_xor(s, 8);
         float mean = s * (1.0f / 128.0f);
         float vs = 0.0f;
 #pragma unroll
-        for (int j = 0; j < 16; j++) { float d = v[j] - mean; vs += d * d; }
-        vs += __shfl_xor(vs, 1); vs += __shfl_xor(vs, 2); vs += __shfl_xor(vs, 4);
+        for (int j = 0; j < 8; j++) { float d = v[j] - mean; vs += d * d; }
+        vs += __shfl_xor(vs, 1); vs += __shfl_xor(vs, 2);
+        vs += __shfl_xor(vs, 4); vs += __shfl_xor(vs, 8);
         float rstd = rsqrtf(vs * (1.0f / 128.0f) + 1e-5f);
 #pragma unroll
-        for (int j = 0; j < 16; j++) {
-            int col = cg * 16 + j;
+        for (int j = 0; j < 8; j++) {
+            int col = cg * 8 + j;
             float y = (v[j] - mean) * rstd * g1[col] + be1[col];
             X1f[row][col] = y;
             X1h[row][col] = (bf16)y;
@@ -465,103 +454,85 @@
     }
     __syncthreads();
     {
+        int cb2 = w * 64;
         bf16x8 af[4];
 #pragma unroll
         for (int k = 0; k < 4; k++)
-            af[k] = *(const bf16x8*)&X1h[r0l + c][k * 32 + gq * 8];
-#pragma unroll
-        for (int ci = 0; ci < 2; ci++) {
-            int cb2 = cb + ci * 128;
-            const bf16x8* Wp0 = (const bf16x8*)(W1 + (size_t)(cb2 + c) * 128) + gq;
-            const bf16x8* Wp1 = (const bf16x8*)(W1 + (size_t)(cb2 + 16 + c) * 128) + gq;
-            const bf16x8* Wp2 = (const bf16x8*)(W1 + (size_t)(cb2 + 32 + c) * 128) + gq;
-            const bf16x8* Wp3 = (const bf16x8*)(W1 + (size_t)(cb2 + 48 + c) * 128) + gq;
-            f32x4 a0 = zero, a1 = zero, a2 = zero, a3 = zero;
-#pragma unroll
-            for (int k = 0; k < 4; k++) {
-                a0 = __builtin_amdgcn_mfma_f32_16x16x32_bf16(af[k], Wp0[k * 4], a0, 0, 0, 0);
-                a1 = __builtin_amdgcn_mfma_f32_16x16x32_bf16(af[k], Wp1[k * 4], a1, 0, 0, 0);
-                a2 = __builtin_amdgcn_mfma_f32_16x16x32_bf16(af[k], Wp2[k * 4], a2, 0, 0, 0);
-                a3 = __builtin_amdgcn_mfma_f32_16x16x32_bf16(af[k], Wp3[k * 4], a3, 0, 0, 0);
-            }
-            int lrow = r0l + gq * 4;
-#pragma unroll
-            for (int r = 0; r < 4; r++) {
-                H[lrow + r][cb2 + c]      = (bf16)gelu_f(a0[r] + bf1[cb2 + c]);
-                H[lrow + r][cb2 + 16 + c] = (bf16)gelu_f(a1[r] + bf1[cb2 + 16 + c]);
-                H[lrow + r][cb2 + 32 + c] = (bf16)gelu_f(a2[r] + bf1[cb2 + 32 + c]);
-                H[lrow + r][cb2 + 48 + c] = (bf16)gelu_f(a3[r] + bf1[cb2 + 48 + c]);
-            }
-        }
-    }
-    __syncthreads();
-    {
-        bf16x8 af[8];
-#pragma unroll
-        for (int k = 0; k < 8; k++)
-            af[k] = *(const bf16x8*)&H[r0l + c][k * 32 + gq * 8];
-        const bf16x8* Wp0 = (const bf16x8*)(W2 + (size_t)(cb + c) * 256) + gq;
-        const bf16x8* Wp1 = (const bf16x8*)(W2 + (size_t)(cb + 16 + c) * 256) + gq;
-        const bf16x8* Wp2 = (const bf16x8*)(W2 + (size_t)(cb + 32 + c) * 256) + gq;
-        const bf16x8* Wp3 = (const bf16x8*)(W2 + (size_t)(cb + 48 + c) * 256) + gq;
+            af[k] = *(const bf16x8*)&X1h[c][k * 32 + gq * 8];
+        const bf16x8* Wp0 = (const bf16x8*)(W1 + (size_t)(cb2 + c) * 128) + gq;
+        const bf16x8* Wp1 = (const bf16x8*)(W1 + (size_t)(cb2 + 16 + c) * 128) + gq;
+        const bf16x8* Wp2 = (const bf16x8*)(W1 + (size_t)(cb2 + 32 + c) * 128) + gq;
+        const bf16x8* Wp3 = (const bf16x8*)(W1 + (size_t)(cb2 + 48 + c) * 128) + gq;
         f32x4 a0 = zero, a1 = zero, a2 = zero, a3 = zero;
 #pragma unroll
-        for (int k = 0; k < 8; k++) {
+        for (int k = 0; k < 4; k++) {
             a0 = __builtin_amdgcn_mfma_f32_16x16x32_bf16(af[k], Wp0[k * 4], a0, 0, 0, 0);
             a1 = __builtin_amdgcn_mfma_f32_16x16x32_bf16(af[k], Wp1[k * 4], a1, 0, 0, 0);
             a2 = __builtin_amdgcn_mfma_f32_16x16x32_bf16(af[k], Wp2[k * 4], a2, 0, 0, 0);
             a3 = __builtin_amdgcn_mfma_f32_16x16x32_bf16(af[k], Wp3[k * 4], a3, 0, 0, 0);
         }
-        int lrow = r0l + gq * 4;
-        float b0 = bf2[cb + c], b1v = bf2[cb + 16 + c];
-        float b2v = bf2[cb + 32 + c], b3v = bf2[cb + 48 + c];
 #pragma unroll
         for (int r = 0; r < 4; r++) {
-            S[lrow + r][cb + c] = a0[r] + b0;
-            S[lrow + r][cb + 16 + c] = a1[r] + b1v;
-            S[lrow + r][cb + 32 + c] = a2[r] + b2v;
-            S[lrow + r][cb + 48 + c] = a3[r] + b3v;
-        }
-    }
-    __syncthreads();
-    {
-        int row = tid >> 3, cg = tid & 7;
-        float v[16];
-#pragma unroll
-        for (int j = 0; j < 16; j++)
-            v[j] = S[row][cg * 16 + j] + X1f[row][cg * 16 + j];
+            H[gq * 4 + r][cb2 + c]      = (bf16)gelu_f(a0[r] + bf1[cb2 + c]);
+            H[gq * 4 + r][cb2 + 16 + c] = (bf16)gelu_f(a1[r] + bf1[cb2 + 16 + c]);
+            H[gq * 4 + r][cb2 + 32 + c] = (bf16)gelu_f(a2[r] + bf1[cb2 + 32 + c]);
+            H[gq * 4 + r][cb2 + 48 + c] = (bf16)gelu_f(a3[r] + bf1[cb2 + 48 + c]);
+        }
+    }
+    __syncthreads();
+    {
+        int cb = w * 32;
+        bf16x8 af[8];
+#pragma unroll
+        for (int k = 0; k < 8; k++)
+            af[k] = *(const bf16x8*)&H[c][k * 32 + gq * 8];
+        const bf16x8* Wp0 = (const bf16x8*)(W2 + (size_t)(cb + c) * 256) + gq;
+        const bf16x8* Wp1 = (const bf16x8*)(W2 + (size_t)(cb + 16 + c) * 256) + gq;
+        f32x4 a0 = zero, a1 = zero;
+#pragma unroll
+        for (int k = 0; k < 8; k++) {
+            a0 = __builtin_amdgcn_mfma_f32_16x16x32_bf16(af[k], Wp0[k * 4], a0, 0, 0, 0);
+            a1 = __builtin_amdgcn_mfma_f32_16x16x32_bf16(af[k], Wp1[k * 4], a1, 0, 0, 0);
+        }
+#pragma unroll
+        for (int r = 0; r < 4; r++) {
+            S[gq * 4 + r][cb + c] = a0[r] + bf2[cb + c];
+            S[gq * 4 + r][cb + 16 + c] = a1[r] + bf2[cb + 16 + c];
+        }
+    }
+    __syncthreads();
+    {
+        int row = tid >> 4, cg = tid & 15;
+        float v[8];
+#pragma unroll
+        for (int j = 0; j < 8; j++)
+            v[j] = S[row][cg * 8 + j] + X1f[row][cg * 8 + j];
         float s = 0.0f;
 #pragma unroll
-        for (int j = 0; j < 16; j++) s += v[j];
-        s += __shfl_xor(s, 1); s += __shfl_xor(s, 2); s += __shfl_xor(s, 4);
+        for (int j = 0; j < 8; j++) s += v[j];
+        s += __shfl_xor(s, 1); s += __shfl_xor(s, 2);
+        s += __shfl_xor(s, 4); s += __shfl_xor(s, 8);
         float mean = s * (1.0f / 128.0f);
         float vs = 0.0f;
 #pragma unroll
-        for (int j = 0; j < 16; j++) { float d = v[j] - mean; vs += d * d; }
-        vs += __shfl_xor(vs, 1); vs += __shfl_xor(vs, 2); vs += __shfl_xor(vs, 4);
+        for (int j = 0; j < 8; j++) { float d = v[j] - mean; vs += d * d; }
+        vs += __shfl_xor(vs, 1); vs += __shfl_xor(vs, 2);
+        vs += __shfl_xor(vs, 4); vs += __shfl_xor(vs, 8);
         float rstd = rsqrtf(vs * (1.0f / 128.0f) + 1e-5f);
-        size_t grow = (size_t)(blk * 32 + row);
-        float4* of = (float4*)(X0out + grow * 128 + cg * 16);
-        bf16x8* oh = (bf16x8*)(X0hout + grow * 128 + cg * 16);
-        float y[16];
-#pragma unroll
-        for (int j = 0; j < 16; j++) {
-            int col = cg * 16 + j;
+        size_t grow = (size_t)(blk * 16 + row);
+        float y[8];
+#pragma unroll
+        for (int j = 0; j < 8; j++) {
+            int col = cg * 8 + j;
             y[j] = (v[j] - mean) * rstd * g2[col] + be2[col];
         }
-#pragma unroll
-        for (int j4 = 0; j4 < 4; j4++) {
-            float4 o; o.x = y[4 * j4]; o.y = y[4 * j4 + 1];
-            o.z = y[4 * j4 + 2]; o.w = y[4 * j4 + 3];
-            of[j4] = o;
-        }
-#pragma unroll
-        for (int j8 = 0; j8 < 2; j8++) {
-            bf16x8 o;
-#pragma unroll
-            for (int e = 0; e < 8; e++) o[e] = (bf16)y[8 * j8 + e];
-            oh[j8] = o;
-        }
+        float4* of = (float4*)(X0out + grow * 128 + cg * 8);
+        of[0] = (float4){y[0], y[1], y[2], y[3]};
+        of[1] = (float4){y[4], y[5], y[6], y[7]};
+        bf16x8 o;
+#pragma unroll
+        for (int e = 0; e < 8; e++) o[e] = (bf16)y[e];
+        *(bf16x8*)(X0hout + grow * 128 + cg * 8) = o;
     }
 }
 
@@ -573,20 +544,18 @@
     const float* __restrict__ bf1, const bf16* __restrict__ W2,
     const float* __restrict__ bf2, const float* __restrict__ g2,
     const float* __restrict__ be2, float* __restrict__ outp) {
-    __shared__ float S[32][132];
-    __shared__ bf16 s1h[32][136];
-    __shared__ bf16 H[32][520];
+    __shared__ float S[16][132];
+    __shared__ bf16 s1h[16][136];
+    __shared__ bf16 H[16][520];
     int tid = threadIdx.x;
     int w = tid >> 6, lane = tid & 63;
     int c = lane & 15, gq = lane >> 4;
-    int r0l = (w >> 1) * 16;
-    int cb = (w & 1) * 64;
     int blk = blockIdx.x;
     const f32x4 zero = {0, 0, 0, 0};
 
     bf16x8 agl[4];
     {
-        int tr = blk * 32 + r0l + c;
+        int tr = blk * 16 + c;
         int b = tr >> 11, t = (tr >> 3) & 255, n = tr & 7;
         const bf16* xrow = X0h + ((size_t)((b * 8 + n) * 256 + t)) * 128;
 #pragma unroll
@@ -595,57 +564,48 @@
     }
 
     {
-        const bf16x8* Ap  = (const bf16x8*)(ATTh + (size_t)(blk * 32 + r0l + c) * 128) + gq;
+        int cb = w * 32;
+        const bf16x8* Ap  = (const bf16x8*)(ATTh + (size_t)(blk * 16 + c) * 128) + gq;
         const bf16x8* Wp0 = (const bf16x8*)(Wo + (size_t)(cb + c) * 128) + gq;
         const bf16x8* Wp1 = (const bf16x8*)(Wo + (size_t)(cb + 16 + c) * 128) + gq;
-        const bf16x8* Wp2 = (const bf16x8*)(Wo + (size_t)(cb + 32 + c) * 128) + gq;
-        const bf16x8* Wp3 = (const bf16x8*)(Wo + (size_t)(cb + 48 + c) * 128) + gq;
-        f32x4 a0 = zero, a1 = zero, a2 = zero, a3 = zero;
+        f32x4 a0 = zero, a1 = zero;
 #pragma unroll
         for (int k = 0; k < 4; k++) {
             bf16x8 av = Ap[k * 4];
             a0 = __builtin_amdgcn_mfma_f32_16x16x32_bf16(av, Wp0[k * 4], a0, 0, 0, 0);
             a1 = __builtin_amdgcn_mfma_f32_16x16x32_bf16(av, Wp1[k * 4], a1, 0, 0, 0);
-            a2 = __builtin_amdgcn_mfma_f32_16x16x32_bf16(av, Wp2[k * 4], a2, 0, 0, 0);
-            a3 = __builtin_amdgcn_mfma_f32_16x16x32_bf16(av, Wp3[k * 4], a3, 0, 0, 0);
-        }
-        int lrow = r0l + gq * 4;
-        float b0 = bo[cb + c], b1v = bo[cb + 16 + c];
-        float b2v = bo[cb + 32 + c], b3v = bo[cb + 48 + c];
+        }
 #pragma unroll
         for (int r = 0; r < 4; r++) {
-            S[lrow + r][cb + c] = a0[r] + b0;
-            S[lrow + r][cb + 16 + c] = a1[r] + b1v;
-            S[lrow + r][cb + 32 + c] = a2[r] + b2v;
-            S[lrow + r][cb + 48 + c] = a3[r] + b3v;
-        }
-    }
-    __syncthreads();
-    {
-        int row = tid >> 3, cg = tid & 7;
-        float v[16];
-        const float4* rp = (const float4*)(semb + (size_t)(blk * 32 + row) * 128 + cg * 16);
-#pragma unroll
-        for (int j4 = 0; j4 < 4; j4++) {
-            float4 rv = rp[j4];
-            v[4 * j4 + 0] = S[row][cg * 16 + 4 * j4 + 0] + rv.x;
-            v[4 * j4 + 1] = S[row][cg * 16 + 4 * j4 + 1] + rv.y;
-            v[4 * j4 + 2] = S[row][cg * 16 + 4 * j4 + 2] + rv.z;
-            v[4 * j4 + 3] = S[row][cg * 16 + 4 * j4 + 3] + rv.w;
-        }
+            S[gq * 4 + r][cb + c] = a0[r] + bo[cb + c];
+            S[gq * 4 + r][cb + 16 + c] = a1[r] + bo[cb + 16 + c];
+        }
+    }
+    __syncthreads();
+    {
+        int row = tid >> 4, cg = tid & 15;
+        float v[8];
+        const float4* rp = (const float4*)(semb + (size_t)(blk * 16 + row) * 128 + cg * 8);
+        float4 r0 = rp[0], r1 = rp[1];
+        v[0] = S[row][cg * 8 + 0] + r0.x; v[1] = S[row][cg * 8 + 1] + r0.y;
+        v[2] = S[row][cg * 8 + 2] + r0.z; v[3] = S[row][cg * 8 + 3] + r0.w;
+        v[4] = S[row][cg * 8 + 4] + r1.x; v[5] = S[row][cg * 8 + 5] + r1.y;
+        v[6] = S[row][cg * 8 + 6] + r1.z; v[7] = S[row][cg * 8 + 7] + r1.w;
         float s = 0.0f;
 #pragma unroll
-        for (int j = 0; j < 16; j++) s += v[j];
-        s += __shfl_xor(s, 1); s += __shfl_xor(s, 2); s += __shfl_xor(s, 4);
+        for (int j = 0; j < 8; j++) s += v[j];
+        s += __shfl_xor(s, 1); s += __shfl_xor(s, 2);
+        s += __shfl_xor(s, 4); s += __shfl_xor(s, 8);
         float mean = s * (1.0f / 128.0f);
         float vs = 0.0f;
 #pragma unroll
-        for (int j = 0; j < 16; j++) { float d = v[j] - mean; vs += d * d; }
-        vs += __shfl_xor(vs, 1); vs += __shfl_xor(vs, 2); vs += __shfl_xor(vs, 4);
+        for (int j = 0; j < 8; j++) { float d = v[j] - mean; vs += d * d; }
+        vs += __shfl_xor(vs, 1); vs += __shfl_xor(vs, 2);
+        vs += __shfl_xor(vs, 4); vs += __shfl_xor(vs, 8);
         float rstd = rsqrtf(vs * (1.0f / 128.0f) + 1e-5f);
 #pragma unroll
-        for (int j = 0; j < 16; j++) {
-            int col = cg * 16 + j;
+        for (int j = 0; j < 8; j++) {
+            int col = cg * 8 + j;
             s1h[row][col] = (bf16)((v[j] - mean) * rstd * g1[col] + be1[col]);
         }
     }
@@ -654,10 +614,10 @@
         bf16x8 afl[4];
 #pragma unroll
         for (int k = 0; k < 4; k++)
-            afl[k] = *(const bf16x8*)&s1h[r0l + c][k * 32 + gq * 8];
-#pragma unroll
-        for (int ci = 0; ci < 4; ci++) {
-            int cb2 = cb + ci * 128;
+            afl[k] = *(const bf16x8*)&s1h[c][k * 32 + gq * 8];
+#pragma unroll
+        for (int ci = 0; ci < 2; ci++) {
+            int cb2 = w * 128 + ci * 64;
             const bf16x8* Wp0 = (const bf16x8*)(W1 + (size_t)(cb2 + c) * 256) + gq;
             const bf16x8* Wp1 = (const bf16x8*)(W1 + (size_t)(cb2 + 16 + c) * 256) + gq;
             const bf16x8* Wp2 = (const bf16x8*)(W1 + (size_t)(cb2 + 32 + c) * 256) + gq;
@@ -671,70 +631,61 @@
                 a2 = __builtin_amdgcn_mfma_f32_16x16x32_bf16(av, Wp2[k * 4], a2, 0, 0, 0);
                 a3 = __builtin_amdgcn_mfma_f32_16x16x32_bf16(av, Wp3[k * 4], a3, 0, 0, 0);
             }
-            int lrow = r0l + gq * 4;
 #pragma unroll
             for (int r = 0; r < 4; r++) {
-                H[lrow + r][cb2 + c]      = (bf16)gelu_f(a0[r] + bf1[cb2 + c]);
-                H[lrow + r][cb2 + 16 + c] = (bf16)gelu_f(a1[r] + bf1[cb2 + 16 + c]);
-                H[lrow + r][cb2 + 32 + c] = (bf16)gelu_f(a2[r] + bf1[cb2 + 32 + c]);
-                H[lrow + r][cb2 + 48 + c] = (bf16)gelu_f(a3[r] + bf1[cb2 + 48 + c]);
+                H[gq * 4 + r][cb2 + c]      = (bf16)gelu_f(a0[r] + bf1[cb2 + c]);
+                H[gq * 4 + r][cb2 + 16 + c] = (bf16)gelu_f(a1[r] + bf1[cb2 + 16 + c]);
+                H[gq * 4 + r][cb2 + 32 + c] = (bf16)gelu_f(a2[r] + bf1[cb2 + 32 + c]);
+                H[gq * 4 + r][cb2 + 48 + c] = (bf16)gelu_f(a3[r] + bf1[cb2 + 48 + c]);
             }
         }
     }
     __syncthreads();
     {
+        int cb = w * 32;
         const bf16x8* Wp0 = (const bf16x8*)(W2 + (size_t)(cb + c) * 512) + gq;
         const bf16x8* Wp1 = (const bf16x8*)(W2 + (size_t)(cb + 16 + c) * 512) + gq;
-        const bf16x8* Wp2 = (const bf16x8*)(W2 + (size_t)(cb + 32 + c) * 512) + gq;
-        const bf16x8* Wp3 = (const bf16x8*)(W2 + (size_t)(cb + 48 + c) * 512) + gq;
-        f32x4 a0 = zero, a1 = zero, a2 = zero, a3 = zero;
+        f32x4 a0 = zero, a1 = zero;
 #pragma unroll
         for (int k = 0; k < 16; k++) {
-            bf16x8 av = *(const bf16x8*)&H[r0l + c][k * 32 + gq * 8];
+            bf16x8 av = *(const bf16x8*)&H[c][k * 32 + gq * 8];
             a0 = __builtin_amdgcn_mfma_f32_16x16x32_bf16(av, Wp0[k * 4], a0, 0, 0, 0);
             a1 = __builtin_amdgcn_mfma_f32_16x16x32_bf16(av, Wp1[k * 4], a1, 0, 0, 0);
-            a2 = __builtin_amdgcn_mfma_f32_16x16x32_bf16(av, Wp2[k * 4], a2, 0, 0, 0);
-            a3 = __builtin_amdgcn_mfma_f32_16x16x32_bf16(av, Wp3[k * 4], a3, 0, 0, 0);
-        }
-        int lrow = r0l + gq * 4;
-        float b0 = bf2[cb + c], b1v = bf2[cb + 16 + c];
-        float b2v = bf2[cb + 32 + c], b3v = bf2[cb + 48 + c];
+        }
 #pragma unroll
         for (int r = 0; r < 4; r++) {
-            S[lrow + r][cb + c] = a0[r] + b0;
-            S[lrow + r][cb + 16 + c] = a1[r] + b1v;
-            S[lrow + r][cb + 32 + c] = a2[r] + b2v;
-            S[lrow + r][cb + 48 + c] = a3[r] + b3v;
-        }
-    }
-    __syncthreads();
-    {
-        int row = tid >> 3, cg = tid & 7;
-        float v[16];
-#pragma unroll
-        for (int j = 0; j < 16; j++)
-            v[j] = S[row][cg * 16 + j] + (float)s1h[row][cg * 16 + j];
+            S[gq * 4 + r][cb + c] = a0[r] + bf2[cb + c];
+            S[gq * 4 + r][cb + 16 + c] = a1[r] + bf2[cb + 16 + c];
+        }
+    }
+    __syncthreads();
+    {
+        int row = tid >> 4, cg = tid & 15;
+        float v[8];
+#pragma unroll
+        for (int j = 0; j < 8; j++)
+            v[j] = S[row][cg * 8 + j] + (float)s1h[row][cg * 8 + j];
         float s = 0.0f;
 #pragma unroll
-        for (int j = 0; j < 16; j++) s += v[j];
-        s += __shfl_xor(s, 1); s += __shfl_xor(s, 2); s += __shfl_xor(s, 4);
+        for (int j = 0; j < 8; j++) s += v[j];
+        s += __shfl_xor(s, 1); s += __shfl_xor(s, 2);
+        s += __shfl_xor(s, 4); s += __shfl_xor(s, 8);
         float mean = s * (1.0f / 128.0f);
         float vs = 0.0f;
 #pragma unroll
-        for (int j = 0; j < 16; j++) { float d = v[j] - mean; vs += d * d; }
-        vs += __shfl_xor(vs, 1); vs += __shfl_xor(vs, 2); vs += __shfl_xor(vs, 4);
+        for (int j = 0; j < 8; j++) { float d = v[j] - mean; vs += d * d; }
+        vs += __shfl_xor(vs, 1); vs += __shfl_xor(vs, 2);
+        vs += __shfl_xor(vs, 4); vs += __shfl_xor(vs, 8);
         float rstd = rsqrtf(vs * (1.0f / 128.0f) + 1e-5f);
-        float4* of = (float4*)(outp + (size_t)(blk * 32 + row) * 128 + cg * 16);
-#pragma unroll
-        for (int j4 = 0; j4 < 4; j4++) {
-            float4 o;
-#pragma unroll
-            for (int e = 0; e < 4; e++) {
-                int col = cg * 16 + 4 * j4 + e;
-                ((float*)&o)[e] = (v[4 * j4 + e] - mean) * rstd * g2[col] + be2[col];
-            }
-            of[j4] = o;
-        }
+        float y[8];
+#pragma unroll
+        for (int j = 0; j < 8; j++) {
+            int col = cg * 8 + j;
+            y[j] = (v[j] - mean) * rstd * g2[col] + be2[col];
+        }
+        float4* of = (float4*)(outp + (size_t)(blk * 16 + (tid >> 4)) * 128 + cg * 8);
+        of[0] = (float4){y[0], y[1], y[2], y[3]};
+        of[1] = (float4){y[4], y[5], y[6], y[7]};
     }
 }
 
@@ -907,14 +858,14 @@
         ca_ff_W1, ca_ff_W2, mlp_W2, semb, ca_bk, ca_bv, Wpk, sembh, bpk,
         vs, r5, A55, bl_bias, nl_W1, nl_b1, nl_W2, nl_b2, b1w);
 
-    k_mlp_ln<<<dim3(256), dim3(256), 0, stream>>>(
+    k_mlp_ln<<<dim3(512), dim3(256), 0, stream>>>(
         vs, b1w, mlp_W1, mlp_b1, Wpk + 524288, mlp_b2, mlp_ln_g, mlp_ln_b,
         X0, X0h);
 
     for (int i = 0; i < LENC_; i++) {
-        k_enc_attn<<<dim3(128), dim3(256), 0, stream>>>(
+        k_enc_attn<<<dim3(256), dim3(256), 0, stream>>>(
             X0h, Wpk + i * 49152, enc_qkv_b + i * 384, ATTh);
-        k_enc_tail<<<dim3(256), dim3(256), 0, stream>>>(
+        k_enc_tail<<<dim3(512), dim3(256), 0, stream>>>(
             ATTh, Wpk + 98304 + i * 16384, enc_out_b + i * 128, X0,
             enc_ln1_g + i * 128, enc_ln1_b + i * 128,
             Wpk + 131072 + i * 32768, enc_ff_b1 + i * 256,
@@ -926,7 +877,7 @@
         sembh, Wpk + 262144, ca_bq, X0h, Wpk + 278528, bpk, Qh, Kh, Vth);
     k_mattn<<<dim3(512), dim3(256), 0, stream>>>(
         Qh, Kh, Vth, ATTh, 2048, 2048, 16);
-    k_cross_tail<<<dim3(256), dim3(256), 0, stream>>>(
+    k_cross_tail<<<dim3(512), dim3(256), 0, stream>>>(
         ATTh, Wpk + 311296, ca_bo, semb, ca_ln1_g, ca_ln1_b, X0h,
         Wpk + 327680, ca_ff_b1, Wpk + 458752, ca_ff_b2,
         ca_ln2_g, ca_ln2_b, out);
```

Measured after the change: 306.1 us. 9.2% less time.
